# Kernel tuning notes

Measured on AMD Instinct MI355X. Metric: run time of the kernel, lower is better.

## Reference

```python
import jax, jax.numpy as jnp
import numpy as np

N_NODES = 2048
N_EDGES = 131072
N_LINE = 524288
D = 128
H = 4
NUM_RBF = 50
CUTOFF = 8.0
N_LAYERS = 4


def setup_inputs() -> dict:
    key = jax.random.key(0)
    ks = iter(jax.random.split(key, 64))
    def nrm(shape, s=0.05):
        return jax.random.normal(next(ks), shape, dtype=jnp.float32) * s
    inp = {}
    inp["atomic_numbers"] = jax.random.randint(next(ks), (N_NODES,), 1, 101)
    inp["positions"] = jax.random.normal(next(ks), (N_NODES, 3), dtype=jnp.float32) * 4.0
    inp["edge_index"] = jax.random.randint(next(ks), (2, N_EDGES), 0, N_NODES)
    inp["line_edge_index"] = jax.random.randint(next(ks), (2, N_LINE), 0, N_EDGES)
    inp["line_angles"] = jax.random.uniform(next(ks), (N_LINE, 1), dtype=jnp.float32) * np.float32(np.pi)
    # embeddings
    inp["atom_table"] = nrm((100, D), 1.0)
    inp["rbf_w1"] = nrm((NUM_RBF, D)); inp["rbf_b1"] = jnp.zeros((D,), jnp.float32)
    inp["rbf_w2"] = nrm((D, D));       inp["rbf_b2"] = jnp.zeros((D,), jnp.float32)
    inp["line_emb_w"] = nrm((1, D), 1.0); inp["line_emb_b"] = jnp.zeros((D,), jnp.float32)
    # per-layer params, stacked over N_LAYERS (weights stored [in,out], used as x @ W + b)
    inp["eu_w1"] = nrm((N_LAYERS, 3 * D, 2 * D)); inp["eu_b1"] = jnp.zeros((N_LAYERS, 2 * D), jnp.float32)
    inp["eu_w2"] = nrm((N_LAYERS, 2 * D, D));     inp["eu_b2"] = jnp.zeros((N_LAYERS, D), jnp.float32)
    inp["lu_w1"] = nrm((N_LAYERS, 2 * D, D));     inp["lu_b1"] = jnp.zeros((N_LAYERS, D), jnp.float32)
    inp["lu_w2"] = nrm((N_LAYERS, D, D));         inp["lu_b2"] = jnp.zeros((N_LAYERS, D), jnp.float32)
    inp["nu_w1"] = nrm((N_LAYERS, 2 * D, 2 * D)); inp["nu_b1"] = jnp.zeros((N_LAYERS, 2 * D), jnp.float32)
    inp["nu_w2"] = nrm((N_LAYERS, 2 * D, D));     inp["nu_b2"] = jnp.zeros((N_LAYERS, D), jnp.float32)
    inp["attn_wqkv"] = nrm((N_LAYERS, D, 3 * D)); inp["attn_bqkv"] = jnp.zeros((N_LAYERS, 3 * D), jnp.float32)
    inp["attn_wo"] = nrm((N_LAYERS, D, D));       inp["attn_bo"] = jnp.zeros((N_LAYERS, D), jnp.float32)
    inp["nn_g"] = jnp.ones((N_LAYERS, D), jnp.float32); inp["nn_b"] = jnp.zeros((N_LAYERS, D), jnp.float32)
    inp["en_g"] = jnp.ones((N_LAYERS, D), jnp.float32); inp["en_b"] = jnp.zeros((N_LAYERS, D), jnp.float32)
    inp["ln_g"] = jnp.ones((N_LAYERS, D), jnp.float32); inp["ln_b"] = jnp.zeros((N_LAYERS, D), jnp.float32)
    # readout
    inp["ro_w1"] = nrm((D, D));      inp["ro_b1"] = jnp.zeros((D,), jnp.float32)
    inp["ro_w2"] = nrm((D, D // 2)); inp["ro_b2"] = jnp.zeros((D // 2,), jnp.float32)
    inp["ro_w3"] = nrm((D // 2, 1)); inp["ro_b3"] = jnp.zeros((1,), jnp.float32)
    return inp


def _layernorm(x, g, b, eps=1e-5):
    m = jnp.mean(x, -1, keepdims=True)
    v = jnp.mean((x - m) ** 2, -1, keepdims=True)
    return (x - m) * jax.lax.rsqrt(v + eps) * g + b


def _seg_mean_num(x, idx, n):
    s = jax.ops.segment_sum(x, idx, num_segments=n)
    c = jax.ops.segment_sum(jnp.ones((idx.shape[0],), x.dtype), idx, num_segments=n)
    return s / jnp.clip(c, 1.0)[:, None]


def alignn_forward(atomic_numbers, positions, edge_index, line_edge_index, line_angles,
                   atom_table, rbf_w1, rbf_b1, rbf_w2, rbf_b2, line_emb_w, line_emb_b,
                   eu_w1, eu_b1, eu_w2, eu_b2, lu_w1, lu_b1, lu_w2, lu_b2,
                   nu_w1, nu_b1, nu_w2, nu_b2, attn_wqkv, attn_bqkv, attn_wo, attn_bo,
                   nn_g, nn_b, en_g, en_b, ln_g, ln_b,
                   ro_w1, ro_b1, ro_w2, ro_b2, ro_w3, ro_b3):
    silu = jax.nn.silu
    src, dst = edge_index[0], edge_index[1]
    lsrc, ldst = line_edge_index[0], line_edge_index[1]
    nN, nE = atomic_numbers.shape[0], src.shape[0]

    # edge distances & embeddings
    vec = positions[dst] - positions[src]                      # [E,3]
    dist = jnp.linalg.norm(vec, axis=-1)                       # [E]
    centers = jnp.linspace(0.0, CUTOFF, NUM_RBF)
    widths = jnp.full((NUM_RBF,), CUTOFF / NUM_RBF, jnp.float32)
    rbf = jnp.exp(-((dist[:, None] - centers) ** 2) / (2.0 * widths ** 2))
    cut = 0.5 * (jnp.cos(dist * jnp.pi / CUTOFF) + 1.0) * (dist < CUTOFF).astype(dist.dtype)
    rbf = rbf * cut[:, None]
    edge = silu(rbf @ rbf_w1 + rbf_b1) @ rbf_w2 + rbf_b2       # [E,D]
    node = atom_table[atomic_numbers - 1]                      # [N,D]
    line = line_angles @ line_emb_w + line_emb_b               # [Lg,D]

    xs = {"eu_w1": eu_w1, "eu_b1": eu_b1, "eu_w2": eu_w2, "eu_b2": eu_b2,
          "lu_w1": lu_w1, "lu_b1": lu_b1, "lu_w2": lu_w2, "lu_b2": lu_b2,
          "nu_w1": nu_w1, "nu_b1": nu_b1, "nu_w2": nu_w2, "nu_b2": nu_b2,
          "wqkv": attn_wqkv, "bqkv": attn_bqkv, "wo": attn_wo, "bo": attn_bo,
          "nn_g": nn_g, "nn_b": nn_b, "en_g": en_g, "en_b": en_b, "ln_g": ln_g, "ln_b": ln_b}

    def step(carry, p):
        node, edge, line = carry
        # line-graph edge update
        li = jnp.concatenate([edge[lsrc], edge[ldst]], -1)     # [Lg,2D]
        lu = silu(li @ p["lu_w1"] + p["lu_b1"]) @ p["lu_w2"] + p["lu_b2"]
        line = _layernorm(line + lu, p["ln_g"], p["ln_b"])
        # aggregate line edges -> edges (mean over dst)
        laggr = _seg_mean_num(line, ldst, nE)                  # [E,D]
        ei = jnp.concatenate([edge, edge, laggr], -1)          # [E,3D]
        eu = silu(ei @ p["eu_w1"] + p["eu_b1"]) @ p["eu_w2"] + p["eu_b2"]
        edge = _layernorm(edge + eu, p["en_g"], p["en_b"])
        # aggregate edges -> nodes (mean over dst)
        naggr = _seg_mean_num(edge, dst, nN)                   # [N,D]
        ni = jnp.concatenate([node, naggr], -1)                # [N,2D]
        nu = silu(ni @ p["nu_w1"] + p["nu_b1"]) @ p["nu_w2"] + p["nu_b2"]
        node = _layernorm(node + nu, p["nn_g"], p["nn_b"])
        # global self-attention over nodes (batch=1, seq=N)
        qkv = node @ p["wqkv"] + p["bqkv"]                     # [N,3D]
        q, k, v = jnp.split(qkv, 3, axis=-1)
        dh = D // H
        q = q.reshape(nN, H, dh); k = k.reshape(nN, H, dh); v = v.reshape(nN, H, dh)
        scores = jnp.einsum("qhd,khd->hqk", q, k) / jnp.sqrt(jnp.float32(dh))
        attn = jax.nn.softmax(scores, axis=-1)
        o = jnp.einsum("hqk,khd->qhd", attn, v).reshape(nN, D)
        node = o @ p["wo"] + p["bo"]
        return (node, edge, line), None

    (node, edge, line), _ = jax.lax.scan(step, (node, edge, line), xs)

    g = node.mean(axis=0, keepdims=True)                       # [1,D]
    h = silu(g @ ro_w1 + ro_b1)
    h = silu(h @ ro_w2 + ro_b2)
    return h @ ro_w3 + ro_b3                                   # [1,1]


def reference(atomic_numbers, positions, edge_index, line_edge_index, line_angles,
              atom_table, rbf_w1, rbf_b1, rbf_w2, rbf_b2, line_emb_w, line_emb_b,
              eu_w1, eu_b1, eu_w2, eu_b2, lu_w1, lu_b1, lu_w2, lu_b2,
              nu_w1, nu_b1, nu_w2, nu_b2, attn_wqkv, attn_bqkv, attn_wo, attn_bo,
              nn_g, nn_b, en_g, en_b, ln_g, ln_b,
              ro_w1, ro_b1, ro_w2, ro_b2, ro_w3, ro_b3):
    return alignn_forward(atomic_numbers, positions, edge_index, line_edge_index, line_angles,
                          atom_table, rbf_w1, rbf_b1, rbf_w2, rbf_b2, line_emb_w, line_emb_b,
                          eu_w1, eu_b1, eu_w2, eu_b2, lu_w1, lu_b1, lu_w2, lu_b2,
                          nu_w1, nu_b1, nu_w2, nu_b2, attn_wqkv, attn_bqkv, attn_wo, attn_bo,
                          nn_g, nn_b, en_g, en_b, ln_g, ln_b,
                          ro_w1, ro_b1, ro_w2, ro_b2, ro_w3, ro_b3)
```

## Files before the change

kernel.cpp:

```cpp
#include <hip/hip_runtime.h>
#include <hip/hip_fp16.h>


#define NN 2048
#define NE 131072
#define NL 524288
#define DM 128

typedef unsigned short u16;
typedef unsigned int uint;
typedef __attribute__((ext_vector_type(8))) _Float16 f16x8;
typedef __attribute__((ext_vector_type(2))) _Float16 f16x2;
typedef __attribute__((ext_vector_type(4))) float f32x4;

__device__ __forceinline__ float h2f(u16 u){ return __half2float(__ushort_as_half(u)); }
__device__ __forceinline__ u16 f2h(float f){ return __half_as_ushort(__float2half(f)); }
__device__ __forceinline__ uint pk2h(float a, float b){
  union { decltype(__builtin_amdgcn_cvt_pkrtz(0.f,0.f)) h2; uint u; } cv;
  cv.h2 = __builtin_amdgcn_cvt_pkrtz(a, b);
  return cv.u;
}
__device__ __forceinline__ float siluf(float x){ return x/(1.f+__expf(-x)); }
__device__ __forceinline__ float4 ld4(const float* p){ return *(const float4*)p; }
__device__ __forceinline__ void fma44(float (&a)[4], float4 x, float4 w0, float4 w1, float4 w2, float4 w3){
  a[0] += x.x*w0.x + x.y*w1.x + x.z*w2.x + x.w*w3.x;
  a[1] += x.x*w0.y + x.y*w1.y + x.z*w2.y + x.w*w3.y;
  a[2] += x.x*w0.z + x.y*w1.z + x.z*w2.z + x.w*w3.z;
  a[3] += x.x*w0.w + x.y*w1.w + x.z*w2.w + x.w*w3.w;
}


__global__ void k_zero2(int* __restrict__ a, int na, int* __restrict__ b, int nb){
  int i = blockIdx.x*256 + threadIdx.x;
  if (i < na) a[i] = 0;
  else if (i - na < nb) b[i - na] = 0;
}

__global__ void k_sentinel(float* out, float wsmb){ out[0] = 1000000.0f + wsmb; }

__global__ void k_einv(const int* __restrict__ perm2, int* __restrict__ einv, int n){
  int i = blockIdx.x*256 + threadIdx.x;
  if (i < n) einv[perm2[i]] = i;
}

__global__ void k_lidx2(const int* __restrict__ lsrc, const int* __restrict__ ldst,
                        const int* __restrict__ perm1, const int* __restrict__ einv,
                        int* __restrict__ lsrc2, int* __restrict__ ldst2, int n){
  int i = blockIdx.x*256 + threadIdx.x;
  if (i < n){
    int o = perm1[i];
    lsrc2[i] = einv[lsrc[o]];
    ldst2[i] = einv[ldst[o]];
  }
}


__global__ __launch_bounds__(256) void k_scanp1(
    const int* __restrict__ inA, int* __restrict__ outA,
    const int* __restrict__ inB, int* __restrict__ outB,
    int* __restrict__ bsumA, int* __restrict__ bsumB){
  __shared__ int wsum[4];
  const int b = blockIdx.x, t = threadIdx.x;
  const int* in;  int* out;  int* bsum;  int base;
  if (b < 64){ in = inA; out = outA; bsum = bsumA + b; base = b*2048; }
  else       { in = inB; out = outB; bsum = bsumB;     base = 0; }
  int v[8];
  int s = 0;
  #pragma unroll
  for (int j=0;j<8;j++){ v[j] = in[base + t*8 + j]; s += v[j]; }
  const int lane = t & 63, wid = t >> 6;
  int x = s;
  #pragma unroll
  for (int off=1; off<64; off<<=1){
    int u = __shfl_up(x, off);
    if (lane >= off) x += u;
  }
  if (lane == 63) wsum[wid] = x;
  __syncthreads();
  int woff = 0;
  #pragma unroll
  for (int i=0;i<3;i++) if (i < wid) woff += wsum[i];
  int run = woff + x - s;
  #pragma unroll
  for (int j=0;j<8;j++){ out[base + t*8 + j] = run; run += v[j]; }
  if (t == 255) *bsum = woff + x;
}

__global__ void k_scanp2(int* __restrict__ bsumA, int* __restrict__ outA, int nA,
                         const int* __restrict__ bsumB, int* __restrict__ outB, int nB){
  __shared__ int sh[64];
  const int t = threadIdx.x;
  if (t < 64) sh[t] = bsumA[t];
  __syncthreads();
  if (t == 0){
    int run = 0;
    for (int i=0;i<64;i++){ int v = sh[i]; sh[i] = run; run += v; }
    outA[nA] = run;
    outB[nB] = bsumB[0];
  }
  __syncthreads();
  if (t < 64) bsumA[t] = sh[t];
}

__global__ __launch_bounds__(256) void k_scanp3(int* __restrict__ outA, const int* __restrict__ bsumA){
  const int b = blockIdx.x;
  const int off = bsumA[b];
  const int base = b*2048 + threadIdx.x*8;
  #pragma unroll
  for (int j=0;j<8;j++) outA[base+j] += off;
}

__global__ void k_wfrag_all(const float* __restrict__ luw1, const float* __restrict__ luw2,
                            const float* __restrict__ euw1, const float* __restrict__ euw2,
                            u16* __restrict__ lw1h, u16* __restrict__ lw2h,
                            u16* __restrict__ ew1h, u16* __restrict__ ew2h){
  int l = blockIdx.x / 72, r = blockIdx.x % 72;
  const float* W; u16* out; int N, total, lb; bool fold = false;
  if (r < 16){      W = luw1 + (size_t)l*256*128; out = lw1h + (size_t)l*32768; N=128; total=4096;  lb = r; }
  else if (r < 24){ W = luw2 + (size_t)l*128*128; out = lw2h + (size_t)l*16384; N=128; total=2048;  lb = r-16; }
  else if (r < 56){ W = euw1 + (size_t)l*384*256; out = ew1h + (size_t)l*65536; N=256; total=8192;  lb = r-24; fold = true; }
  else {            W = euw2 + (size_t)l*256*128; out = ew2h + (size_t)l*32768; N=128; total=4096;  lb = r-56; }
  int i = lb*256 + threadIdx.x;
  if (i >= total) return;
  int lane = i & 63;
  int frag = i >> 6;
  int NT = N >> 4;
  int ntg = frag % NT;
  int kt = frag / NT;
  int half = NT >> 1;
  int colh = ntg / half, j = ntg % half;
  int col  = colh*(half<<4) + ((j>>1)<<5) + 2*(lane&15) + (j&1);
  int row0 = kt*32 + (lane>>4)*8;
  uint4 v; uint* vp = (uint*)&v;
  #pragma unroll
  for (int p=0;p<4;p++){
    int ra = row0+2*p, rb = row0+2*p+1;
    float fa, fb;
    if (fold){
      fa = (ra < 128) ? W[(size_t)ra*N + col] + W[(size_t)(ra+128)*N + col]
                      : W[(size_t)(ra+128)*N + col];
      fb = (rb < 128) ? W[(size_t)rb*N + col] + W[(size_t)(rb+128)*N + col]
                      : W[(size_t)(rb+128)*N + col];
    } else {
      fa = W[(size_t)ra*N + col];
      fb = W[(size_t)rb*N + col];
    }
    vp[p] = (uint)f2h(fa) | ((uint)f2h(fb)<<16);
  }
  *(uint4*)(out + (size_t)i*8) = v;
}

__global__ void k_rbf_wfrag(const float* __restrict__ rw1, const float* __restrict__ rw2,
                            u16* __restrict__ w1p, u16* __restrict__ w2p){
  int r = blockIdx.x;
  const float* W; u16* out; int K, total;
  if (r < 4){ W = rw1; out = w1p; K = 50;  total = 1024; }
  else      { W = rw2; out = w2p; K = 128; total = 2048; r -= 4; }
  int i = r*256 + threadIdx.x;
  if (i >= total) return;
  int lane = i & 63, frag = i >> 6;
  int ntg = frag % 8, kt = frag / 8;
  int colh = ntg / 4, j = ntg % 4;
  int col  = colh*64 + ((j>>1)<<5) + 2*(lane&15) + (j&1);
  int row0 = kt*32 + (lane>>4)*8;
  uint4 v; uint* vp = (uint*)&v;
  #pragma unroll
  for (int p=0;p<4;p++){
    int ra = row0+2*p, rb = row0+2*p+1;
    u16 a = (ra < K) ? f2h(W[(size_t)ra*128 + col]) : (u16)0;
    u16 b = (rb < K) ? f2h(W[(size_t)rb*128 + col]) : (u16)0;
    vp[p] = (uint)a | ((uint)b<<16);
  }
  *(uint4*)(out + (size_t)i*8) = v;
}


__global__ void k_node_init(const int* __restrict__ an, const float* __restrict__ tab, float* __restrict__ node){
  int i = blockIdx.x*256 + threadIdx.x;
  int n = i >> 7, d = i & 127;
  node[i] = tab[(an[n]-1)*DM + d];
}

__global__ void k_line_init(const float* __restrict__ ang, const float* __restrict__ w,
                            const float* __restrict__ b, const int* __restrict__ perm1,
                            u16* __restrict__ line){
  int i = blockIdx.x*256 + threadIdx.x;
  int r = i >> 6; int c2 = (i & 63)*2;
  float a = ang[perm1[r]];
  ushort2 v;
  v.x = f2h(a*w[c2  ] + b[c2  ]);
  v.y = f2h(a*w[c2+1] + b[c2+1]);
  ((ushort2*)line)[i] = v;
}

#define EB_RS 72
#define EB_HS 136

__global__ __launch_bounds__(256) void k_edge_embed2(
    const float* __restrict__ pos, const int* __restrict__ eidx,
    const int* __restrict__ eperm,
    const u16* __restrict__ W1p, const float* __restrict__ B1,
    const u16* __restrict__ W2p, const float* __restrict__ B2,
    u16* __restrict__ edge){
  __shared__ __align__(16) u16 rs[32*EB_RS];
  __shared__ __align__(16) u16 hs[32*EB_HS];
  __shared__ float dsh[32];
  const int t = threadIdx.x;
  const int e0 = blockIdx.x*32;
  if (t < 32){
    int eo = eperm[e0 + t];
    int s = eidx[eo], d = eidx[NE + eo];
    float dx = pos[d*3+0]-pos[s*3+0];
    float dy = pos[d*3+1]-pos[s*3+1];
    float dz = pos[d*3+2]-pos[s*3+2];
    dsh[t] = sqrtf(dx*dx+dy*dy+dz*dz);
  }
  __syncthreads();
  for (int q = t; q < 32*64; q += 256){
    int m = q >> 6, k = q & 63;
    float d = dsh[m];
    float v = 0.f;
    if (k < 50){
      float c = 8.0f*(float)k/49.0f;
      float g = __expf(-(d-c)*(d-c)*19.53125f);
      float cut = (d < 8.0f) ? 0.5f*(__cosf(d*0.39269908169872414f)+1.0f) : 0.0f;
      v = g*cut;
    }
    rs[m*EB_RS + k] = f2h(v);
  }
  __syncthreads();

  const int lane = t & 63, w = t >> 6;
  const int band = w >> 1, colh = w & 1;
  const int arow = band*16 + (lane & 15);
  const int kgrp = (lane >> 4)*8;
  const int q2 = 2*(lane & 15);

  {
    f32x4 acc[4];
    #pragma unroll
    for (int nt=0; nt<4; ++nt){
      float bv = B1[colh*64 + (nt>>1)*32 + q2 + (nt&1)];
      acc[nt][0]=bv; acc[nt][1]=bv; acc[nt][2]=bv; acc[nt][3]=bv;
    }
    #pragma unroll
    for (int kt=0; kt<2; ++kt){
      f16x8 a = *(const f16x8*)(rs + arow*EB_RS + kt*32 + kgrp);
      #pragma unroll
      for (int nt=0; nt<4; ++nt){
        int ntg = colh*4 + nt;
        f16x8 b = *(const f16x8*)(W1p + ((size_t)(kt*8 + ntg)*64 + lane)*8);
        acc[nt] = __builtin_amdgcn_mfma_f32_16x16x32_f16(a, b, acc[nt], 0, 0, 0);
      }
    }
    #pragma unroll
    for (int p=0; p<2; ++p){
      int colb = colh*64 + p*32 + q2;
      #pragma unroll
      for (int r=0; r<4; ++r){
        int row = band*16 + (lane>>4)*4 + r;
        *(uint*)(hs + row*EB_HS + colb) = pk2h(siluf(acc[2*p][r]), siluf(acc[2*p+1][r]));
      }
    }
  }
  __syncthreads();
  {
    f32x4 acc[4];
    #pragma unroll
    for (int nt=0; nt<4; ++nt){
      float bv = B2[colh*64 + (nt>>1)*32 + q2 + (nt&1)];
      acc[nt][0]=bv; acc[nt][1]=bv; acc[nt][2]=bv; acc[nt][3]=bv;
    }
    #pragma unroll
    for (int kt=0; kt<4; ++kt){
      f16x8 a = *(const f16x8*)(hs + arow*EB_HS + kt*32 + kgrp);
      #pragma unroll
      for (int nt=0; nt<4; ++nt){
        int ntg = colh*4 + nt;
        f16x8 b = *(const f16x8*)(W2p + ((size_t)(kt*8 + ntg)*64 + lane)*8);
        acc[nt] = __builtin_amdgcn_mfma_f32_16x16x32_f16(a, b, acc[nt], 0, 0, 0);
      }
    }
    #pragma unroll
    for (int p=0; p<2; ++p){
      int colb = colh*64 + p*32 + q2;
      #pragma unroll
      for (int r=0; r<4; ++r){
        int row = band*16 + (lane>>4)*4 + r;
        *(uint*)(edge + (size_t)(e0+row)*DM + colb) = pk2h(acc[2*p][r], acc[2*p+1][r]);
      }
    }
  }
}


__global__ void k_hist2(const int* __restrict__ idxA, int* __restrict__ histA,
                        const int* __restrict__ idxB, int* __restrict__ histB, int nblkA){
  int t = threadIdx.x;
  if ((int)blockIdx.x < nblkA){
    int i = blockIdx.x*256 + t;
    atomicAdd(&histA[idxA[i]], 1);
  } else {
    int i = (blockIdx.x - nblkA)*256 + t;
    atomicAdd(&histB[idxB[i]], 1);
  }
}

__global__ void k_perm2k(const int* __restrict__ idxA, const int* __restrict__ baseA,
                         int* __restrict__ curA, int* __restrict__ permA,
                         const int* __restrict__ idxB, const int* __restrict__ baseB,
                         int* __restrict__ curB, int* __restrict__ permB, int nblkA){
  int t = threadIdx.x;
  if ((int)blockIdx.x < nblkA){
    int i = blockIdx.x*256 + t;
    int e = idxA[i];
    int p = atomicAdd(&curA[e], 1);
    permA[baseA[e] + p] = i;
  } else {
    int i = (blockIdx.x - nblkA)*256 + t;
    int e = idxB[i];
    int p = atomicAdd(&curB[e], 1);
    permB[baseB[e] + p] = i;
  }
}


#define PE_XS 136

__global__ __launch_bounds__(256) void k_pre_lu(
    const u16* __restrict__ edge, const u16* __restrict__ W1h,
    u16* __restrict__ A16, u16* __restrict__ Bm16){
  __shared__ __align__(16) u16 xs[32*PE_XS];
  const int t = threadIdx.x;
  const int r0 = blockIdx.x*32;
  #pragma unroll
  for (int it=0; it<2; ++it){
    int idx = it*256 + t;
    int m = idx >> 4, c = idx & 15;
    uint4 v = *(const uint4*)(edge + (size_t)(r0+m)*DM + c*8);
    *(uint4*)(xs + m*PE_XS + c*8) = v;
  }
  __syncthreads();
  const int lane = t & 63, w = t >> 6;
  const int band = w >> 1, colh = w & 1;
  const int arow = band*16 + (lane & 15);
  const int kgrp = (lane >> 4)*8;
  const int q2 = 2*(lane & 15);
  #pragma unroll
  for (int half=0; half<2; ++half){
    f32x4 acc[4];
    #pragma unroll
    for (int nt=0; nt<4; ++nt){ acc[nt][0]=0.f; acc[nt][1]=0.f; acc[nt][2]=0.f; acc[nt][3]=0.f; }
    #pragma unroll
    for (int kt=0; kt<4; ++kt){
      f16x8 a = *(const f16x8*)(xs + arow*PE_XS + kt*32 + kgrp);
      #pragma unroll
      for (int nt=0; nt<4; ++nt){
        int ntg = colh*4 + nt;
        f16x8 b = *(const f16x8*)(W1h + ((size_t)((kt + half*4)*8 + ntg)*64 + lane)*8);
        acc[nt] = __builtin_amdgcn_mfma_f32_16x16x32_f16(a, b, acc[nt], 0, 0, 0);
      }
    }
    u16* out = half ? Bm16 : A16;
    #pragma unroll
    for (int p=0; p<2; ++p){
      int colb = colh*64 + p*32 + q2;
      #pragma unroll
      for (int r=0; r<4; ++r){
        int row = band*16 + (lane>>4)*4 + r;
        *(uint*)(out + (size_t)(r0+row)*DM + colb) = pk2h(acc[2*p][r], acc[2*p+1][r]);
      }
    }
  }
}


#define LU_HS 136
#define LU_OS 132

__global__ __launch_bounds__(256) void k_lu2(
    const u16* __restrict__ A16, const u16* __restrict__ Bm16,
    const int* __restrict__ lsrc2, const int* __restrict__ ldst2,
    const float* __restrict__ B1,
    const u16* __restrict__ W2h, const float* __restrict__ B2,
    const float* __restrict__ lg, const float* __restrict__ lb,
    u16* __restrict__ line){
  __shared__ __align__(16) float smem[32*LU_OS];
  u16* hs = (u16*)smem;
  const int t = threadIdx.x;
  const int r0 = blockIdx.x*32;

  {
    int m = t >> 3, c8 = t & 7;
    int r = r0 + m;
    const u16* ap = A16  + (size_t)lsrc2[r]*DM;
    const u16* bp = Bm16 + (size_t)ldst2[r]*DM;
    #pragma unroll
    for (int cc0=0; cc0<2; ++cc0){
      int cc = c8 + cc0*8;
      uint4 av = *(const uint4*)(ap + cc*8);
      uint4 bv = *(const uint4*)(bp + cc*8);
      const __half2* ah = (const __half2*)&av;
      const __half2* bh = (const __half2*)&bv;
      uint outw[4];
      #pragma unroll
      for (int p=0;p<4;p++){
        int col = cc*8 + 2*p;
        __half2 b1v = __floats2half2_rn(B1[col], B1[col+1]);
        __half2 x2 = __hadd2(__hadd2(ah[p], bh[p]), b1v);
        float x0 = __half2float(__low2half(x2));
        float x1 = __half2float(__high2half(x2));
        outw[p] = pk2h(siluf(x0), siluf(x1));
      }
      *(uint4*)(hs + m*LU_HS + cc*8) = *(uint4*)outw;
    }
  }
  __syncthreads();

  const int lane = t & 63, w = t >> 6;
  const int band = w >> 1, colh = w & 1;
  const int arow = band*16 + (lane & 15);
  const int kgrp = (lane >> 4)*8;
  const int q2 = 2*(lane & 15);

  f32x4 acc[4];
  #pragma unroll
  for (int nt=0; nt<4; ++nt){
    float bv = B2[colh*64 + (nt>>1)*32 + q2 + (nt&1)];
    acc[nt][0]=bv; acc[nt][1]=bv; acc[nt][2]=bv; acc[nt][3]=bv;
  }
  #pragma unroll
  for (int kt=0; kt<4; ++kt){
    f16x8 a = *(const f16x8*)(hs + arow*LU_HS + kt*32 + kgrp);
    #pragma unroll
    for (int nt=0; nt<4; ++nt){
      int ntg = colh*4 + nt;
      f16x8 b = *(const f16x8*)(W2h + ((size_t)(kt*8 + ntg)*64 + lane)*8);
      acc[nt] = __builtin_amdgcn_mfma_f32_16x16x32_f16(a, b, acc[nt], 0, 0, 0);
    }
  }
  __syncthreads();
  #pragma unroll
  for (int p=0; p<2; ++p){
    int colb = colh*64 + p*32 + q2;
    #pragma unroll
    for (int r=0; r<4; ++r){
      int row = band*16 + (lane>>4)*4 + r;
      *(float2*)(smem + row*LU_OS + colb) = make_float2(acc[2*p][r], acc[2*p+1][r]);
    }
  }
  __syncthreads();
  {
    const float* outp = (const float*)smem;
    int row = t >> 3, li = t & 7;
    size_t rb = (size_t)(r0 + row)*DM;
    uint rw[8];
    *(uint4*)&rw[0] = *(const uint4*)(line + rb + li*16);
    *(uint4*)&rw[4] = *(const uint4*)(line + rb + li*16 + 8);
    float x[16];
    float s=0.f, q=0.f;
    #pragma unroll
    for (int j=0;j<16;j++){
      float res = h2f((u16)((j&1) ? (rw[j>>1]>>16) : (rw[j>>1]&0xffffu)));
      x[j] = outp[row*LU_OS + li*16 + j] + res;
      s += x[j]; q += x[j]*x[j];
    }
    #pragma unroll
    for (int off=1; off<8; off<<=1){ s += __shfl_xor(s,off); q += __shfl_xor(q,off); }
    float mean = s*(1.f/128.f);
    float rstd = rsqrtf(fmaxf(q*(1.f/128.f) - mean*mean, 0.f) + 1e-5f);
    #pragma unroll
    for (int half=0; half<2; ++half){
      uint4 wv; uint* wp = (uint*)&wv;
      #pragma unroll
      for (int p=0;p<4;p++){
        int j = half*8 + 2*p;
        int c0 = li*16 + j;
        wp[p] = pk2h((x[j  ]-mean)*rstd*lg[c0  ] + lb[c0  ],
                     (x[j+1]-mean)*rstd*lg[c0+1] + lb[c0+1]);
      }
      *(uint4*)(line + rb + li*16 + half*8) = wv;
    }
  }
}


#define EU_XS 264
#define EU_HS 264
#define EU_OS 132

__global__ __launch_bounds__(256) void k_eu_mfma(
    const u16* __restrict__ W1h, const float* __restrict__ B1,
    const u16* __restrict__ W2h, const float* __restrict__ B2,
    const float* __restrict__ g, const float* __restrict__ bb,
    u16* __restrict__ edge, const u16* __restrict__ line,
    const int* __restrict__ lbase, const int* __restrict__ eperm){
  __shared__ __align__(16) u16 xs[32*EU_XS];
  __shared__ __align__(16) u16 hs[32*EU_HS];
  const int t = threadIdx.x;
  const int r0 = blockIdx.x*32;

  for (int it=0; it<2; ++it){
    int idx = it*256 + t;
    int m = idx >> 4, c = idx & 15;
    uint4 v = *(const uint4*)(edge + (size_t)(r0+m)*DM + c*8);
    *(uint4*)(xs + m*EU_XS + c*8) = v;
  }
  {
    int m = t >> 3, c0 = (t & 7)*16;
    int eo = eperm[r0 + m];
    int b0 = lbase[eo], b1 = lbase[eo+1];
    float s[16];
    #pragma unroll
    for (int k=0;k<16;k++) s[k]=0.f;
    for (int j=b0;j<b1;++j){
      const u16* lp = line + (size_t)j*DM + c0;
      uint rw[8];
      *(uint4*)&rw[0] = *(const uint4*)lp;
      *(uint4*)&rw[4] = *(const uint4*)(lp + 8);
      #pragma unroll
      for (int k=0;k<16;k++)
        s[k] += h2f((u16)((k&1) ? (rw[k>>1]>>16) : (rw[k>>1]&0xffffu)));
    }
    int n = b1 - b0;
    float inv = 1.f/(float)(n > 0 ? n : 1);
    #pragma unroll
    for (int half=0; half<2; ++half){
      uint4 wv; uint* wp = (uint*)&wv;
      #pragma unroll
      for (int p=0;p<4;p++){
        int k = half*8 + 2*p;
        wp[p] = pk2h(s[k]*inv, s[k+1]*inv);
      }
      *(uint4*)(xs + m*EU_XS + 128 + c0 + half*8) = wv;
    }
  }
  __syncthreads();

  const int lane = t & 63, w = t >> 6;
  const int band = w >> 1, colh = w & 1;
  const int arow = band*16 + (lane & 15);
  const int kgrp = (lane >> 4)*8;
  const int q2 = 2*(lane & 15);

  {
    f32x4 acc[8];
    #pragma unroll
    for (int nt=0; nt<8; ++nt){
      float bv = B1[colh*128 + (nt>>1)*32 + q2 + (nt&1)];
      acc[nt][0]=bv; acc[nt][1]=bv; acc[nt][2]=bv; acc[nt][3]=bv;
    }
    #pragma unroll
    for (int kt=0; kt<8; ++kt){
      f16x8 a = *(const f16x8*)(xs + arow*EU_XS + kt*32 + kgrp);
      #pragma unroll
      for (int nt=0; nt<8; ++nt){
        int ntg = colh*8 + nt;
        f16x8 b = *(const f16x8*)(W1h + ((size_t)(kt*16 + ntg)*64 + lane)*8);
        acc[nt] = __builtin_amdgcn_mfma_f32_16x16x32_f16(a, b, acc[nt], 0, 0, 0);
      }
    }
    #pragma unroll
    for (int p=0; p<4; ++p){
      int colb = colh*128 + p*32 + q2;
      #pragma unroll
      for (int r=0; r<4; ++r){
        int row = band*16 + (lane>>4)*4 + r;
        *(uint*)(hs + row*EU_HS + colb) = pk2h(siluf(acc[2*p][r]), siluf(acc[2*p+1][r]));
      }
    }
  }
  __syncthreads();
  {
    f32x4 acc[4];
    #pragma unroll
    for (int nt=0; nt<4; ++nt){
      float bv = B2[colh*64 + (nt>>1)*32 + q2 + (nt&1)];
      acc[nt][0]=bv; acc[nt][1]=bv; acc[nt][2]=bv; acc[nt][3]=bv;
    }
    #pragma unroll
    for (int kt=0; kt<8; ++kt){
      f16x8 a = *(const f16x8*)(hs + arow*EU_HS + kt*32 + kgrp);
      #pragma unroll
      for (int nt=0; nt<4; ++nt){
        int ntg = colh*4 + nt;
        f16x8 b = *(const f16x8*)(W2h + ((size_t)(kt*8 + ntg)*64 + lane)*8);
        acc[nt] = __builtin_amdgcn_mfma_f32_16x16x32_f16(a, b, acc[nt], 0, 0, 0);
      }
    }
    float* outp = (float*)xs;
    #pragma unroll
    for (int p=0; p<2; ++p){
      int colb = colh*64 + p*32 + q2;
      #pragma unroll
      for (int r=0; r<4; ++r){
        int row = band*16 + (lane>>4)*4 + r;
        *(float2*)(outp + row*EU_OS + colb) = make_float2(acc[2*p][r], acc[2*p+1][r]);
      }
    }
  }
  __syncthreads();
  {
    const float* outp = (const float*)xs;
    int row = t >> 3, li = t & 7;
    size_t rb = (size_t)(r0 + row)*DM;
    uint rw[8];
    *(uint4*)&rw[0] = *(const uint4*)(edge + rb + li*16);
    *(uint4*)&rw[4] = *(const uint4*)(edge + rb + li*16 + 8);
    float x[16];
    float s=0.f, q=0.f;
    #pragma unroll
    for (int j=0;j<16;j++){
      float res = h2f((u16)((j&1) ? (rw[j>>1]>>16) : (rw[j>>1]&0xffffu)));
      x[j] = outp[row*EU_OS + li*16 + j] + res;
      s += x[j]; q += x[j]*x[j];
    }
    #pragma unroll
    for (int off=1; off<8; off<<=1){ s += __shfl_xor(s,off); q += __shfl_xor(q,off); }
    float mean = s*(1.f/128.f);
    float rstd = rsqrtf(fmaxf(q*(1.f/128.f) - mean*mean, 0.f) + 1e-5f);
    #pragma unroll
    for (int half=0; half<2; ++half){
      uint4 wv; uint* wp = (uint*)&wv;
      #pragma unroll
      for (int p=0;p<4;p++){
        int j = half*8 + 2*p;
        int c0 = li*16 + j;
        wp[p] = pk2h((x[j  ]-mean)*rstd*g[c0  ] + bb[c0  ],
                     (x[j+1]-mean)*rstd*g[c0+1] + bb[c0+1]);
      }
      *(uint4*)(edge + rb + li*16 + half*8) = wv;
    }
  }
}


template<int KIN>
__global__ __launch_bounds__(256) void k_nu(
    const float* __restrict__ W1, const float* __restrict__ B1,
    const float* __restrict__ W2, const float* __restrict__ B2,
    const float* __restrict__ g, const float* __restrict__ bb,
    float* __restrict__ node_io, const u16* __restrict__ edge,
    const int* __restrict__ nbase){
  __shared__ __align__(16) float xsf[16*KIN];
  __shared__ __align__(16) float hsf[16*256];
  const int t = threadIdx.x;
  const int r0 = blockIdx.x*16;

  {
    int m = t >> 4, c0 = (t & 15)*8;
    int n = r0 + m;
    float4 a = ld4(node_io + (size_t)n*DM + c0);
    float4 b = ld4(node_io + (size_t)n*DM + c0 + 4);
    float* xd = &xsf[m*KIN + c0];
    xd[0]=a.x; xd[1]=a.y; xd[2]=a.z; xd[3]=a.w;
    xd[4]=b.x; xd[5]=b.y; xd[6]=b.z; xd[7]=b.w;
    int b0 = nbase[n], b1e = nbase[n+1];
    float s[8];
    #pragma unroll
    for (int k=0;k<8;k++) s[k]=0.f;
    for (int j=b0;j<b1e;++j){
      uint4 v = *(const uint4*)(edge + (size_t)j*DM + c0);
      s[0]+=h2f((u16)(v.x&0xffff)); s[1]+=h2f((u16)(v.x>>16));
      s[2]+=h2f((u16)(v.y&0xffff)); s[3]+=h2f((u16)(v.y>>16));
      s[4]+=h2f((u16)(v.z&0xffff)); s[5]+=h2f((u16)(v.z>>16));
      s[6]+=h2f((u16)(v.w&0xffff)); s[7]+=h2f((u16)(v.w>>16));
    }
    int nn = b1e - b0;
    float inv = 1.f/(float)(nn > 0 ? nn : 1);
    #pragma unroll
    for (int k=0;k<8;k++) xsf[m*KIN + 128 + c0 + k] = s[k]*inv;
  }
  __syncthreads();
  {
    const int c4 = (t & 63)*4, mg = t >> 6;
    float acc[4][4];
    float4 bv = ld4(B1 + c4);
    #pragma unroll
    for (int i=0;i<4;i++){ acc[i][0]=bv.x; acc[i][1]=bv.y; acc[i][2]=bv.z; acc[i][3]=bv.w; }
    for (int k=0;k<KIN;k+=4){
      float4 w0 = ld4(W1 + (k  )*256 + c4);
      float4 w1 = ld4(W1 + (k+1)*256 + c4);
      float4 w2 = ld4(W1 + (k+2)*256 + c4);
      float4 w3 = ld4(W1 + (k+3)*256 + c4);
      #pragma unroll
      for (int i=0;i<4;i++){
        float4 x = *(const float4*)&xsf[(mg*4+i)*KIN + k];
        fma44(acc[i], x, w0, w1, w2, w3);
      }
    }
    #pragma unroll
    for (int i=0;i<4;i++)
      #pragma unroll
      for (int j=0;j<4;j++)
        hsf[(mg*4+i)*256 + c4 + j] = siluf(acc[i][j]);
  }
  __syncthreads();
  const int c4b = (t & 31)*4, mgb = t >> 5;
  float acc2[2][4];
  {
    float4 bv = ld4(B2 + c4b);
    #pragma unroll
    for (int i=0;i<2;i++){ acc2[i][0]=bv.x; acc2[i][1]=bv.y; acc2[i][2]=bv.z; acc2[i][3]=bv.w; }
    for (int k=0;k<256;k+=4){
      float4 w0 = ld4(W2 + (k  )*128 + c4b);
      float4 w1 = ld4(W2 + (k+1)*128 + c4b);
      float4 w2 = ld4(W2 + (k+2)*128 + c4b);
      float4 w3 = ld4(W2 + (k+3)*128 + c4b);
      #pragma unroll
      for (int i=0;i<2;i++){
        float4 x = *(const float4*)&hsf[(mgb*2+i)*256 + k];
        fma44(acc2[i], x, w0, w1, w2, w3);
      }
    }
  }
  __syncthreads();
  #pragma unroll
  for (int i=0;i<2;i++){
    int m = mgb*2 + i;
    #pragma unroll
    for (int j=0;j<4;j++)
      hsf[m*128 + c4b + j] = acc2[i][j] + xsf[m*KIN + c4b + j];
  }
  __syncthreads();
  {
    int row = t >> 4, li = t & 15;
    const float* o = &hsf[row*128];
    float s=0.f, q=0.f;
    #pragma unroll
    for (int j=0;j<8;j++){ float x = o[li*8+j]; s += x; q += x*x; }
    #pragma unroll
    for (int off=1; off<16; off<<=1){ s += __shfl_xor(s,off); q += __shfl_xor(q,off); }
    float mean = s*(1.f/128.f);
    float rstd = rsqrtf(fmaxf(q*(1.f/128.f) - mean*mean, 0.f) + 1e-5f);
    size_t rb = (size_t)(r0 + row)*DM;
    #pragma unroll
    for (int j=0;j<8;j++){
      int c = li*8 + j;
      node_io[rb + c] = (o[c]-mean)*rstd*g[c] + bb[c];
    }
  }
}


__global__ void k_qkv_split(const float* __restrict__ node, const float* __restrict__ W,
                            const float* __restrict__ B, float* __restrict__ Q,
                            u16* __restrict__ K4, u16* __restrict__ V4){
  int i = blockIdx.x*256 + threadIdx.x;
  int n = i / 384, c = i % 384;
  float acc = B[c];
  const float* nr = node + (size_t)n*DM;
  for (int k=0;k<128;k+=4){
    acc += nr[k  ]*W[(k  )*384+c];
    acc += nr[k+1]*W[(k+1)*384+c];
    acc += nr[k+2]*W[(k+2)*384+c];
    acc += nr[k+3]*W[(k+3)*384+c];
  }
  if (c < 128){
    Q[(size_t)n*128 + c] = acc;
  } else if (c < 256){
    int h = (c-128) >> 5, d = (c-128) & 31;
    K4[((size_t)h*NN + n)*32 + d] = f2h(acc);
  } else {
    int h = (c-256) >> 5, d = (c-256) & 31;
    V4[((size_t)h*NN + n)*32 + d] = f2h(acc);
  }
}

#define AT_TK 128
#define AT_RU 17

__global__ __launch_bounds__(256) void k_attn3(
    const float* __restrict__ Q, const u16* __restrict__ K4,
    const u16* __restrict__ V4, float* __restrict__ attno){
  __shared__ uint kls[2][AT_TK*AT_RU];
  __shared__ uint vls[2][AT_TK*AT_RU];
  const int t = threadIdx.x, lane = t & 63;
  const int h = blockIdx.x >> 8;
  const int q0 = (blockIdx.x & 255)*8 + (t >> 6)*2;
  const float scale = 0.17677669529663687f;
  const uint* Kg = (const uint*)(K4 + (size_t)h*NN*32);
  const uint* Vg = (const uint*)(V4 + (size_t)h*NN*32);
  const int ca = t*2, cb = t*2+1;
  const int ka_ = ca>>2, pa_ = (ca&3)*4;
  const int kb_ = cb>>2, pb_ = (cb&3)*4;
  uint4 kr0, kr1, vr0, vr1;

  f16x2 qh[2][16];
  #pragma unroll
  for (int j=0;j<2;j++){
    const float* qr = Q + (size_t)(q0+j)*128 + h*32;
    #pragma unroll
    for (int u=0;u<16;u++){
      union { uint u32; f16x2 h2; } cv;
      cv.u32 = pk2h(qr[2*u]*scale, qr[2*u+1]*scale);
      qh[j][u] = cv.h2;
    }
  }
  float mx = -1e30f, s0 = 0.f, s1 = 0.f;
  float o0[32], o1[32];
  #pragma unroll
  for (int d=0;d<32;d++){ o0[d]=0.f; o1[d]=0.f; }

  {
    const uint* kg = Kg; const uint* vg = Vg;
    kr0 = *(const uint4*)(kg + ca*4); kr1 = *(const uint4*)(kg + cb*4);
    vr0 = *(const uint4*)(vg + ca*4); vr1 = *(const uint4*)(vg + cb*4);
    uint* kd = kls[0]; uint* vd = vls[0];
    kd[ka_*AT_RU+pa_  ]=kr0.x; kd[ka_*AT_RU+pa_+1]=kr0.y; kd[ka_*AT_RU+pa_+2]=kr0.z; kd[ka_*AT_RU+pa_+3]=kr0.w;
    kd[kb_*AT_RU+pb_  ]=kr1.x; kd[kb_*AT_RU+pb_+1]=kr1.y; kd[kb_*AT_RU+pb_+2]=kr1.z; kd[kb_*AT_RU+pb_+3]=kr1.w;
    vd[ka_*AT_RU+pa_  ]=vr0.x; vd[ka_*AT_RU+pa_+1]=vr0.y; vd[ka_*AT_RU+pa_+2]=vr0.z; vd[ka_*AT_RU+pa_+3]=vr0.w;
    vd[kb_*AT_RU+pb_  ]=vr1.x; vd[kb_*AT_RU+pb_+1]=vr1.y; vd[kb_*AT_RU+pb_+2]=vr1.z; vd[kb_*AT_RU+pb_+3]=vr1.w;
  }
  __syncthreads();

  const int NT = NN / AT_TK;
  for (int kt=0; kt<NT; ++kt){
    if (kt+1 < NT){
      const uint* kg = Kg + (size_t)(kt+1)*AT_TK*16;
      const uint* vg = Vg + (size_t)(kt+1)*AT_TK*16;
      kr0 = *(const uint4*)(kg + ca*4); kr1 = *(const uint4*)(kg + cb*4);
      vr0 = *(const uint4*)(vg + ca*4); vr1 = *(const uint4*)(vg + cb*4);
    }
    {
      const uint* kb = kls[kt&1];
      const uint* vb = vls[kt&1];
      const uint* krA = kb + lane*AT_RU;
      const uint* krB = kb + (lane+64)*AT_RU;
      float dA0=0.f, dA1=0.f, dB0=0.f, dB1=0.f;
      #pragma unroll
      for (int u=0;u<16;u++){
        union { uint u32; f16x2 h2; } ka, kbv;
        ka.u32  = krA[u];
        kbv.u32 = krB[u];
        dA0 = __builtin_amdgcn_fdot2(ka.h2,  qh[0][u], dA0, false);
        dA1 = __builtin_amdgcn_fdot2(ka.h2,  qh[1][u], dA1, false);
        dB0 = __builtin_amdgcn_fdot2(kbv.h2, qh[0][u], dB0, false);
        dB1 = __builtin_amdgcn_fdot2(kbv.h2, qh[1][u], dB1, false);
      }
      float nm = fmaxf(mx, fmaxf(fmaxf(dA0,dA1), fmaxf(dB0,dB1)));
      float r  = __expf(mx - nm);
      mx = nm;
      float eA0 = __expf(dA0 - nm), eA1 = __expf(dA1 - nm);
      float eB0 = __expf(dB0 - nm), eB1 = __expf(dB1 - nm);
      s0 = s0*r + eA0 + eB0;
      s1 = s1*r + eA1 + eB1;
      const uint* vrA = vb + lane*AT_RU;
      const uint* vrB = vb + (lane+64)*AT_RU;
      #pragma unroll
      for (int u=0;u<16;u++){
        uint wA = vrA[u], wB = vrB[u];
        float aA = h2f((u16)(wA&0xffffu)), bA = h2f((u16)(wA>>16));
        float aB = h2f((u16)(wB&0xffffu)), bB = h2f((u16)(wB>>16));
        o0[2*u  ] = o0[2*u  ]*r + eA0*aA + eB0*aB;
        o0[2*u+1] = o0[2*u+1]*r + eA0*bA + eB0*bB;
        o1[2*u  ] = o1[2*u  ]*r + eA1*aA + eB1*aB;
        o1[2*u+1] = o1[2*u+1]*r + eA1*bA + eB1*bB;
      }
    }
    __syncthreads();
    if (kt+1 < NT){
      uint* kd = kls[(kt+1)&1]; uint* vd = vls[(kt+1)&1];
      kd[ka_*AT_RU+pa_  ]=kr0.x; kd[ka_*AT_RU+pa_+1]=kr0.y; kd[ka_*AT_RU+pa_+2]=kr0.z; kd[ka_*AT_RU+pa_+3]=kr0.w;
      kd[kb_*AT_RU+pb_  ]=kr1.x; kd[kb_*AT_RU+pb_+1]=kr1.y; kd[kb_*AT_RU+pb_+2]=kr1.z; kd[kb_*AT_RU+pb_+3]=kr1.w;
      vd[ka_*AT_RU+pa_  ]=vr0.x; vd[ka_*AT_RU+pa_+1]=vr0.y; vd[ka_*AT_RU+pa_+2]=vr0.z; vd[ka_*AT_RU+pa_+3]=vr0.w;
      vd[kb_*AT_RU+pb_  ]=vr1.x; vd[kb_*AT_RU+pb_+1]=vr1.y; vd[kb_*AT_RU+pb_+2]=vr1.z; vd[kb_*AT_RU+pb_+3]=vr1.w;
      __syncthreads();
    }
  }

  #pragma unroll
  for (int off=1; off<64; off<<=1){
    float m2  = __shfl_xor(mx, off);
    float s02 = __shfl_xor(s0, off);
    float s12 = __shfl_xor(s1, off);
    float nm = fmaxf(mx, m2);
    float ra = __expf(mx - nm), rb = __expf(m2 - nm);
    s0 = s0*ra + s02*rb;
    s1 = s1*ra + s12*rb;
    #pragma unroll
    for (int d=0;d<32;d++){
      float a0 = __shfl_xor(o0[d], off);
      float a1 = __shfl_xor(o1[d], off);
      o0[d] = o0[d]*ra + a0*rb;
      o1[d] = o1[d]*ra + a1*rb;
    }
    mx = nm;
  }
  float inv0 = 1.f/s0, inv1 = 1.f/s1;
  if (lane == 0){
    #pragma unroll
    for (int d=0;d<32;d++){
      attno[(size_t)(q0  )*DM + h*32 + d] = o0[d]*inv0;
      attno[(size_t)(q0+1)*DM + h*32 + d] = o1[d]*inv1;
    }
  }
}

__global__ void k_wo(const float* __restrict__ attno, const float* __restrict__ W,
                     const float* __restrict__ B, float* __restrict__ node){
  int i = blockIdx.x*256 + threadIdx.x;
  int n = i >> 7, c = i & 127;
  float acc = B[c];
  const float* ar = attno + (size_t)n*DM;
  for (int k=0;k<128;k+=4){
    acc += ar[k  ]*W[(k  )*128+c];
    acc += ar[k+1]*W[(k+1)*128+c];
    acc += ar[k+2]*W[(k+2)*128+c];
    acc += ar[k+3]*W[(k+3)*128+c];
  }
  node[i] = acc;
}


__global__ __launch_bounds__(256) void k_readout(
    const float* __restrict__ node,
    const float* __restrict__ w1, const float* __restrict__ b1,
    const float* __restrict__ w2, const float* __restrict__ b2,
    const float* __restrict__ w3, const float* __restrict__ b3,
    float* __restrict__ out){
  __shared__ float gs[128], h1[128], h2[64];
  const int t = threadIdx.x;
  if (t < 128){
    float s = 0.f;
    for (int r=0;r<NN;r++) s += node[(size_t)r*DM + t];
    gs[t] = s*(1.f/2048.f);
  }
  __syncthreads();
  if (t < 128){
    float acc = b1[t];
    for (int k=0;k<128;k++) acc += gs[k]*w1[k*128+t];
    h1[t] = siluf(acc);
  }
  __syncthreads();
  if (t < 64){
    float acc = b2[t];
    for (int k=0;k<128;k++) acc += h1[k]*w2[k*64+t];
    h2[t] = siluf(acc);
  }
  __syncthreads();
  if (t == 0){
    float acc = b3[0];
    for (int k=0;k<64;k++) acc += h2[k]*w3[k];
    out[0] = acc;
  }
}


extern "C" void kernel_launch(void* const* d_in, const int* in_sizes, int n_in,
                              void* d_out, int out_size, void* d_ws, size_t ws_size,
                              hipStream_t stream) {
  (void)in_sizes; (void)n_in; (void)out_size;
  const int*   an    = (const int*)  d_in[0];
  const float* pos   = (const float*)d_in[1];
  const int*   eidx  = (const int*)  d_in[2];
  const int*   lidx  = (const int*)  d_in[3];
  const float* lang  = (const float*)d_in[4];
  const float* atab  = (const float*)d_in[5];
  const float* rw1   = (const float*)d_in[6];
  const float* rb1   = (const float*)d_in[7];
  const float* rw2   = (const float*)d_in[8];
  const float* rb2   = (const float*)d_in[9];
  const float* lew   = (const float*)d_in[10];
  const float* leb   = (const float*)d_in[11];
  const float* euw1  = (const float*)d_in[12];
  const float* eub1  = (const float*)d_in[13];
  const float* euw2  = (const float*)d_in[14];
  const float* eub2  = (const float*)d_in[15];
  const float* luw1  = (const float*)d_in[16];
  const float* lub1  = (const float*)d_in[17];
  const float* luw2  = (const float*)d_in[18];
  const float* lub2  = (const float*)d_in[19];
  const float* nuw1  = (const float*)d_in[20];
  const float* nub1  = (const float*)d_in[21];
  const float* nuw2  = (const float*)d_in[22];
  const float* nub2  = (const float*)d_in[23];
  const float* wqkv  = (const float*)d_in[24];
  const float* bqkv  = (const float*)d_in[25];
  const float* wo    = (const float*)d_in[26];
  const float* bo    = (const float*)d_in[27];
  const float* nng   = (const float*)d_in[28];
  const float* nnb   = (const float*)d_in[29];
  const float* eng   = (const float*)d_in[30];
  const float* enb   = (const float*)d_in[31];
  const float* lng   = (const float*)d_in[32];
  const float* lnb   = (const float*)d_in[33];
  const float* row1  = (const float*)d_in[34];
  const float* rob1  = (const float*)d_in[35];
  const float* row2  = (const float*)d_in[36];
  const float* rob2  = (const float*)d_in[37];
  const float* row3  = (const float*)d_in[38];
  const float* rob3  = (const float*)d_in[39];

  char* p = (char*)d_ws;
  auto bump = [&](size_t bytes)->char*{ char* q = p; p += (bytes + 255) & ~(size_t)255; return q; };
  float* node  = (float*)bump((size_t)NN*DM*4);
  float* Q     = (float*)bump((size_t)NN*128*4);
  u16*   K4    = (u16*)  bump((size_t)4*NN*32*2);
  u16*   V4    = (u16*)  bump((size_t)4*NN*32*2);
  float* attno = (float*)bump((size_t)NN*DM*4);
  u16*   edge  = (u16*)  bump((size_t)NE*DM*2);
  u16*   line  = (u16*)  bump((size_t)NL*DM*2);
  u16*   A16   = (u16*)  bump((size_t)NE*DM*2);
  u16*   Bm16  = (u16*)  bump((size_t)NE*DM*2);
  int*   base1 = (int*)  bump((size_t)(NE+1)*4);
  int*   base2 = (int*)  bump((size_t)(NN+1)*4);
  int*   cur1  = (int*)  bump((size_t)NE*4);
  int*   cur2  = (int*)  bump((size_t)NN*4);
  int*   perm1 = (int*)  bump((size_t)NL*4);
  int*   perm2 = (int*)  bump((size_t)NE*4);
  int*   einv  = (int*)  bump((size_t)NE*4);
  int*   lsrc2 = (int*)  bump((size_t)NL*4);
  int*   ldst2 = (int*)  bump((size_t)NL*4);
  int*   bsumA = (int*)  bump((size_t)64*4);
  int*   bsumB = (int*)  bump((size_t)4);
  u16*   lw1h  = (u16*)  bump((size_t)4*32768*2);
  u16*   lw2h  = (u16*)  bump((size_t)4*16384*2);
  u16*   ew1h  = (u16*)  bump((size_t)4*65536*2);
  u16*   ew2h  = (u16*)  bump((size_t)4*32768*2);
  u16*   rw1p  = (u16*)  bump((size_t)8192*2);
  u16*   rw2p  = (u16*)  bump((size_t)16384*2);
  size_t needed = (size_t)(p - (char*)d_ws);
  if (needed > ws_size){
    k_sentinel<<<1, 1, 0, stream>>>((float*)d_out, (float)(ws_size >> 20));
    return;
  }

  const int* lsrc = lidx;
  const int* ldst = lidx + NL;
  const int* dst  = eidx + NE;

  const int nblkA = NL/256, nblkB = NE/256;
  k_zero2<<<(NE+NN+255)/256, 256, 0, stream>>>(cur1, NE, cur2, NN);
  k_hist2<<<nblkA+nblkB, 256, 0, stream>>>(ldst, cur1, dst, cur2, nblkA);
  k_scanp1<<<65, 256, 0, stream>>>(cur1, base1, cur2, base2, bsumA, bsumB);
  k_scanp2<<<1, 64, 0, stream>>>(bsumA, base1, NE, bsumB, base2, NN);
  k_scanp3<<<64, 256, 0, stream>>>(base1, bsumA);
  k_zero2<<<(NE+NN+255)/256, 256, 0, stream>>>(cur1, NE, cur2, NN);
  k_perm2k<<<nblkA+nblkB, 256, 0, stream>>>(ldst, base1, cur1, perm1,
                                            dst,  base2, cur2, perm2, nblkA);
  k_einv<<<(NE+255)/256, 256, 0, stream>>>(perm2, einv, NE);
  k_lidx2<<<(NL+255)/256, 256, 0, stream>>>(lsrc, ldst, perm1, einv, lsrc2, ldst2, NL);

  k_wfrag_all<<<4*72, 256, 0, stream>>>(luw1, luw2, euw1, euw2, lw1h, lw2h, ew1h, ew2h);
  k_rbf_wfrag<<<12, 256, 0, stream>>>(rw1, rw2, rw1p, rw2p);

  k_node_init<<<NN*DM/256, 256, 0, stream>>>(an, atab, node);
  k_line_init<<<NL*64/256, 256, 0, stream>>>(lang, lew, leb, perm1, line);
  k_edge_embed2<<<NE/32, 256, 0, stream>>>(pos, eidx, perm2, rw1p, rb1, rw2p, rb2, edge);

  for (int l=0; l<4; ++l){
    k_pre_lu<<<NE/32, 256, 0, stream>>>(edge, lw1h + (size_t)l*32768, A16, Bm16);
    k_lu2<<<NL/32, 256, 0, stream>>>(A16, Bm16, lsrc2, ldst2,
        lub1 + l*128, lw2h + (size_t)l*16384, lub2 + l*128,
        lng + l*128, lnb + l*128, line);
    k_eu_mfma<<<NE/32, 256, 0, stream>>>(
        ew1h + (size_t)l*65536, eub1 + l*256,
        ew2h + (size_t)l*32768, eub2 + l*128,
        eng + l*128, enb + l*128, edge, line, base1, perm2);
    k_nu<256><<<NN/16, 256, 0, stream>>>(
        nuw1 + (size_t)l*256*256, nub1 + l*256, nuw2 + (size_t)l*256*128, nub2 + l*128,
        nng + l*128, nnb + l*128, node, edge, base2);
    k_qkv_split<<<NN*384/256, 256, 0, stream>>>(node, wqkv + (size_t)l*128*384, bqkv + l*384,
        Q, K4, V4);
    k_attn3<<<1024, 256, 0, stream>>>(Q, K4, V4, attno);
    k_wo<<<NN*DM/256, 256, 0, stream>>>(attno, wo + (size_t)l*128*128, bo + l*128, node);
  }

  k_readout<<<1, 256, 0, stream>>>(node, row1, rob1, row2, rob2, row3, rob3, (float*)d_out);
}
```

Baseline: 1.834 ms.

## Co-schedule next layer's line/edge updates with current layer's attention in merged launches

Kernel bodies become device functions, and combined kernels (k_qp, k_la, k_we) dispatch by block index. Each one runs the node-attention stage of layer l alongside the line and edge update stages of layer l+1, which depend only on edge and line state. This fills the GPU during the small attention kernels and removes launch gaps. The risk is that the merged kernels take the register and shared-memory footprint of their heaviest part, which can reduce occupancy for the larger line and edge work.

```diff
diff --git a/kernel.cpp b/kernel.cpp
--- a/kernel.cpp
+++ b/kernel.cpp
@@ -326,13 +326,13 @@
 
 
 #define PE_XS 136
-
-__global__ __launch_bounds__(256) void k_pre_lu(
+#define PE_SMEM (32*PE_XS*2)
+
+__device__ __forceinline__ void dev_pre_lu(int bid,
     const u16* __restrict__ edge, const u16* __restrict__ W1h,
-    u16* __restrict__ A16, u16* __restrict__ Bm16){
-  __shared__ __align__(16) u16 xs[32*PE_XS];
+    u16* __restrict__ A16, u16* __restrict__ Bm16, u16* xs){
   const int t = threadIdx.x;
-  const int r0 = blockIdx.x*32;
+  const int r0 = bid*32;
   #pragma unroll
   for (int it=0; it<2; ++it){
     int idx = it*256 + t;
@@ -374,9 +374,443 @@
   }
 }
 
-
 #define LU_HS 136
 #define LU_OS 132
+#define LU_SMEM (32*LU_OS*4)
+
+__device__ __forceinline__ void dev_lu2(int bid,
+    const u16* __restrict__ A16, const u16* __restrict__ Bm16,
+    const int* __restrict__ lsrc2, const int* __restrict__ ldst2,
+    const float* __restrict__ B1,
+    const u16* __restrict__ W2h, const float* __restrict__ B2,
+    const float* __restrict__ lg, const float* __restrict__ lb,
+    u16* __restrict__ line, float* smem){
+  u16* hs = (u16*)smem;
+  const int t = threadIdx.x;
+  const int r0 = bid*32;
+
+  {
+    int m = t >> 3, c8 = t & 7;
+    int r = r0 + m;
+    const u16* ap = A16  + (size_t)lsrc2[r]*DM;
+    const u16* bp = Bm16 + (size_t)ldst2[r]*DM;
+    #pragma unroll
+    for (int cc0=0; cc0<2; ++cc0){
+      int cc = c8 + cc0*8;
+      uint4 av = *(const uint4*)(ap + cc*8);
+      uint4 bv = *(const uint4*)(bp + cc*8);
+      const __half2* ah = (const __half2*)&av;
+      const __half2* bh = (const __half2*)&bv;
+      uint outw[4];
+      #pragma unroll
+      for (int p=0;p<4;p++){
+        int col = cc*8 + 2*p;
+        __half2 b1v = __floats2half2_rn(B1[col], B1[col+1]);
+        __half2 x2 = __hadd2(__hadd2(ah[p], bh[p]), b1v);
+        float x0 = __half2float(__low2half(x2));
+        float x1 = __half2float(__high2half(x2));
+        outw[p] = pk2h(siluf(x0), siluf(x1));
+      }
+      *(uint4*)(hs + m*LU_HS + cc*8) = *(uint4*)outw;
+    }
+  }
+  __syncthreads();
+
+  const int lane = t & 63, w = t >> 6;
+  const int band = w >> 1, colh = w & 1;
+  const int arow = band*16 + (lane & 15);
+  const int kgrp = (lane >> 4)*8;
+  const int q2 = 2*(lane & 15);
+
+  f32x4 acc[4];
+  #pragma unroll
+  for (int nt=0; nt<4; ++nt){
+    float bv = B2[colh*64 + (nt>>1)*32 + q2 + (nt&1)];
+    acc[nt][0]=bv; acc[nt][1]=bv; acc[nt][2]=bv; acc[nt][3]=bv;
+  }
+  #pragma unroll
+  for (int kt=0; kt<4; ++kt){
+    f16x8 a = *(const f16x8*)(hs + arow*LU_HS + kt*32 + kgrp);
+    #pragma unroll
+    for (int nt=0; nt<4; ++nt){
+      int ntg = colh*4 + nt;
+      f16x8 b = *(const f16x8*)(W2h + ((size_t)(kt*8 + ntg)*64 + lane)*8);
+      acc[nt] = __builtin_amdgcn_mfma_f32_16x16x32_f16(a, b, acc[nt], 0, 0, 0);
+    }
+  }
+  __syncthreads();
+  #pragma unroll
+  for (int p=0; p<2; ++p){
+    int colb = colh*64 + p*32 + q2;
+    #pragma unroll
+    for (int r=0; r<4; ++r){
+      int row = band*16 + (lane>>4)*4 + r;
+      *(float2*)(smem + row*LU_OS + colb) = make_float2(acc[2*p][r], acc[2*p+1][r]);
+    }
+  }
+  __syncthreads();
+  {
+    const float* outp = (const float*)smem;
+    int row = t >> 3, li = t & 7;
+    size_t rb = (size_t)(r0 + row)*DM;
+    uint rw[8];
+    *(uint4*)&rw[0] = *(const uint4*)(line + rb + li*16);
+    *(uint4*)&rw[4] = *(const uint4*)(line + rb + li*16 + 8);
+    float x[16];
+    float s=0.f, q=0.f;
+    #pragma unroll
+    for (int j=0;j<16;j++){
+      float res = h2f((u16)((j&1) ? (rw[j>>1]>>16) : (rw[j>>1]&0xffffu)));
+      x[j] = outp[row*LU_OS + li*16 + j] + res;
+      s += x[j]; q += x[j]*x[j];
+    }
+    #pragma unroll
+    for (int off=1; off<8; off<<=1){ s += __shfl_xor(s,off); q += __shfl_xor(q,off); }
+    float mean = s*(1.f/128.f);
+    float rstd = rsqrtf(fmaxf(q*(1.f/128.f) - mean*mean, 0.f) + 1e-5f);
+    #pragma unroll
+    for (int half=0; half<2; ++half){
+      uint4 wv; uint* wp = (uint*)&wv;
+      #pragma unroll
+      for (int p=0;p<4;p++){
+        int j = half*8 + 2*p;
+        int c0 = li*16 + j;
+        wp[p] = pk2h((x[j  ]-mean)*rstd*lg[c0  ] + lb[c0  ],
+                     (x[j+1]-mean)*rstd*lg[c0+1] + lb[c0+1]);
+      }
+      *(uint4*)(line + rb + li*16 + half*8) = wv;
+    }
+  }
+}
+
+#define EU_XS 264
+#define EU_HS 264
+#define EU_OS 132
+#define EU_SMEM (32*EU_XS*2 + 32*EU_HS*2)
+
+__device__ __forceinline__ void dev_eu(int bid,
+    const u16* __restrict__ W1h, const float* __restrict__ B1,
+    const u16* __restrict__ W2h, const float* __restrict__ B2,
+    const float* __restrict__ g, const float* __restrict__ bb,
+    u16* __restrict__ edge, const u16* __restrict__ line,
+    const int* __restrict__ lbase, const int* __restrict__ eperm,
+    u16* xs, u16* hs){
+  const int t = threadIdx.x;
+  const int r0 = bid*32;
+
+  for (int it=0; it<2; ++it){
+    int idx = it*256 + t;
+    int m = idx >> 4, c = idx & 15;
+    uint4 v = *(const uint4*)(edge + (size_t)(r0+m)*DM + c*8);
+    *(uint4*)(xs + m*EU_XS + c*8) = v;
+  }
+  {
+    int m = t >> 3, c0 = (t & 7)*16;
+    int eo = eperm[r0 + m];
+    int b0 = lbase[eo], b1 = lbase[eo+1];
+    float s[16];
+    #pragma unroll
+    for (int k=0;k<16;k++) s[k]=0.f;
+    for (int j=b0;j<b1;++j){
+      const u16* lp = line + (size_t)j*DM + c0;
+      uint rw[8];
+      *(uint4*)&rw[0] = *(const uint4*)lp;
+      *(uint4*)&rw[4] = *(const uint4*)(lp + 8);
+      #pragma unroll
+      for (int k=0;k<16;k++)
+        s[k] += h2f((u16)((k&1) ? (rw[k>>1]>>16) : (rw[k>>1]&0xffffu)));
+    }
+    int n = b1 - b0;
+    float inv = 1.f/(float)(n > 0 ? n : 1);
+    #pragma unroll
+    for (int half=0; half<2; ++half){
+      uint4 wv; uint* wp = (uint*)&wv;
+      #pragma unroll
+      for (int p=0;p<4;p++){
+        int k = half*8 + 2*p;
+        wp[p] = pk2h(s[k]*inv, s[k+1]*inv);
+      }
+      *(uint4*)(xs + m*EU_XS + 128 + c0 + half*8) = wv;
+    }
+  }
+  __syncthreads();
+
+  const int lane = t & 63, w = t >> 6;
+  const int band = w >> 1, colh = w & 1;
+  const int arow = band*16 + (lane & 15);
+  const int kgrp = (lane >> 4)*8;
+  const int q2 = 2*(lane & 15);
+
+  {
+    f32x4 acc[8];
+    #pragma unroll
+    for (int nt=0; nt<8; ++nt){
+      float bv = B1[colh*128 + (nt>>1)*32 + q2 + (nt&1)];
+      acc[nt][0]=bv; acc[nt][1]=bv; acc[nt][2]=bv; acc[nt][3]=bv;
+    }
+    #pragma unroll
+    for (int kt=0; kt<8; ++kt){
+      f16x8 a = *(const f16x8*)(xs + arow*EU_XS + kt*32 + kgrp);
+      #pragma unroll
+      for (int nt=0; nt<8; ++nt){
+        int ntg = colh*8 + nt;
+        f16x8 b = *(const f16x8*)(W1h + ((size_t)(kt*16 + ntg)*64 + lane)*8);
+        acc[nt] = __builtin_amdgcn_mfma_f32_16x16x32_f16(a, b, acc[nt], 0, 0, 0);
+      }
+    }
+    #pragma unroll
+    for (int p=0; p<4; ++p){
+      int colb = colh*128 + p*32 + q2;
+      #pragma unroll
+      for (int r=0; r<4; ++r){
+        int row = band*16 + (lane>>4)*4 + r;
+        *(uint*)(hs + row*EU_HS + colb) = pk2h(siluf(acc[2*p][r]), siluf(acc[2*p+1][r]));
+      }
+    }
+  }
+  __syncthreads();
+  {
+    f32x4 acc[4];
+    #pragma unroll
+    for (int nt=0; nt<4; ++nt){
+      float bv = B2[colh*64 + (nt>>1)*32 + q2 + (nt&1)];
+      acc[nt][0]=bv; acc[nt][1]=bv; acc[nt][2]=bv; acc[nt][3]=bv;
+    }
+    #pragma unroll
+    for (int kt=0; kt<8; ++kt){
+      f16x8 a = *(const f16x8*)(hs + arow*EU_HS + kt*32 + kgrp);
+      #pragma unroll
+      for (int nt=0; nt<4; ++nt){
+        int ntg = colh*4 + nt;
+        f16x8 b = *(const f16x8*)(W2h + ((size_t)(kt*8 + ntg)*64 + lane)*8);
+        acc[nt] = __builtin_amdgcn_mfma_f32_16x16x32_f16(a, b, acc[nt], 0, 0, 0);
+      }
+    }
+    float* outp = (float*)xs;
+    #pragma unroll
+    for (int p=0; p<2; ++p){
+      int colb = colh*64 + p*32 + q2;
+      #pragma unroll
+      for (int r=0; r<4; ++r){
+        int row = band*16 + (lane>>4)*4 + r;
+        *(float2*)(outp + row*EU_OS + colb) = make_float2(acc[2*p][r], acc[2*p+1][r]);
+      }
+    }
+  }
+  __syncthreads();
+  {
+    const float* outp = (const float*)xs;
+    int row = t >> 3, li = t & 7;
+    size_t rb = (size_t)(r0 + row)*DM;
+    uint rw[8];
+    *(uint4*)&rw[0] = *(const uint4*)(edge + rb + li*16);
+    *(uint4*)&rw[4] = *(const uint4*)(edge + rb + li*16 + 8);
+    float x[16];
+    float s=0.f, q=0.f;
+    #pragma unroll
+    for (int j=0;j<16;j++){
+      float res = h2f((u16)((j&1) ? (rw[j>>1]>>16) : (rw[j>>1]&0xffffu)));
+      x[j] = outp[row*EU_OS + li*16 + j] + res;
+      s += x[j]; q += x[j]*x[j];
+    }
+    #pragma unroll
+    for (int off=1; off<8; off<<=1){ s += __shfl_xor(s,off); q += __shfl_xor(q,off); }
+    float mean = s*(1.f/128.f);
+    float rstd = rsqrtf(fmaxf(q*(1.f/128.f) - mean*mean, 0.f) + 1e-5f);
+    #pragma unroll
+    for (int half=0; half<2; ++half){
+      uint4 wv; uint* wp = (uint*)&wv;
+      #pragma unroll
+      for (int p=0;p<4;p++){
+        int j = half*8 + 2*p;
+        int c0 = li*16 + j;
+        wp[p] = pk2h((x[j  ]-mean)*rstd*g[c0  ] + bb[c0  ],
+                     (x[j+1]-mean)*rstd*g[c0+1] + bb[c0+1]);
+      }
+      *(uint4*)(edge + rb + li*16 + half*8) = wv;
+    }
+  }
+}
+
+__device__ __forceinline__ void dev_qkv(int bid,
+    const float* __restrict__ node, const float* __restrict__ W,
+    const float* __restrict__ B, float* __restrict__ Q,
+    u16* __restrict__ K4, u16* __restrict__ V4){
+  int i = bid*256 + threadIdx.x;
+  int n = i / 384, c = i % 384;
+  float acc = B[c];
+  const float* nr = node + (size_t)n*DM;
+  for (int k=0;k<128;k+=4){
+    acc += nr[k  ]*W[(k  )*384+c];
+    acc += nr[k+1]*W[(k+1)*384+c];
+    acc += nr[k+2]*W[(k+2)*384+c];
+    acc += nr[k+3]*W[(k+3)*384+c];
+  }
+  if (c < 128){
+    Q[(size_t)n*128 + c] = acc;
+  } else if (c < 256){
+    int h = (c-128) >> 5, d = (c-128) & 31;
+    K4[((size_t)h*NN + n)*32 + d] = f2h(acc);
+  } else {
+    int h = (c-256) >> 5, d = (c-256) & 31;
+    V4[((size_t)h*NN + n)*32 + d] = f2h(acc);
+  }
+}
+
+#define AT_TK 128
+#define AT_RU 17
+#define AT_SMEM (4*AT_TK*AT_RU*4)
+
+__device__ __forceinline__ void dev_attn(int bid,
+    const float* __restrict__ Q, const u16* __restrict__ K4,
+    const u16* __restrict__ V4, float* __restrict__ attno,
+    uint* kls, uint* vls){
+  const int t = threadIdx.x, lane = t & 63;
+  const int h = bid >> 8;
+  const int q0 = (bid & 255)*8 + (t >> 6)*2;
+  const float scale = 0.17677669529663687f;
+  const uint* Kg = (const uint*)(K4 + (size_t)h*NN*32);
+  const uint* Vg = (const uint*)(V4 + (size_t)h*NN*32);
+  const int ca = t*2, cb = t*2+1;
+  const int ka_ = ca>>2, pa_ = (ca&3)*4;
+  const int kb_ = cb>>2, pb_ = (cb&3)*4;
+  uint4 kr0, kr1, vr0, vr1;
+
+  f16x2 qh[2][16];
+  #pragma unroll
+  for (int j=0;j<2;j++){
+    const float* qr = Q + (size_t)(q0+j)*128 + h*32;
+    #pragma unroll
+    for (int u=0;u<16;u++){
+      union { uint u32; f16x2 h2; } cv;
+      cv.u32 = pk2h(qr[2*u]*scale, qr[2*u+1]*scale);
+      qh[j][u] = cv.h2;
+    }
+  }
+  float mx = -1e30f, s0 = 0.f, s1 = 0.f;
+  float o0[32], o1[32];
+  #pragma unroll
+  for (int d=0;d<32;d++){ o0[d]=0.f; o1[d]=0.f; }
+
+  {
+    const uint* kg = Kg; const uint* vg = Vg;
+    kr0 = *(const uint4*)(kg + ca*4); kr1 = *(const uint4*)(kg + cb*4);
+    vr0 = *(const uint4*)(vg + ca*4); vr1 = *(const uint4*)(vg + cb*4);
+    uint* kd = kls; uint* vd = vls;
+    kd[ka_*AT_RU+pa_  ]=kr0.x; kd[ka_*AT_RU+pa_+1]=kr0.y; kd[ka_*AT_RU+pa_+2]=kr0.z; kd[ka_*AT_RU+pa_+3]=kr0.w;
+    kd[kb_*AT_RU+pb_  ]=kr1.x; kd[kb_*AT_RU+pb_+1]=kr1.y; kd[kb_*AT_RU+pb_+2]=kr1.z; kd[kb_*AT_RU+pb_+3]=kr1.w;
+    vd[ka_*AT_RU+pa_  ]=vr0.x; vd[ka_*AT_RU+pa_+1]=vr0.y; vd[ka_*AT_RU+pa_+2]=vr0.z; vd[ka_*AT_RU+pa_+3]=vr0.w;
+    vd[kb_*AT_RU+pb_  ]=vr1.x; vd[kb_*AT_RU+pb_+1]=vr1.y; vd[kb_*AT_RU+pb_+2]=vr1.z; vd[kb_*AT_RU+pb_+3]=vr1.w;
+  }
+  __syncthreads();
+
+  const int NT = NN / AT_TK;
+  for (int kt=0; kt<NT; ++kt){
+    if (kt+1 < NT){
+      const uint* kg = Kg + (size_t)(kt+1)*AT_TK*16;
+      const uint* vg = Vg + (size_t)(kt+1)*AT_TK*16;
+      kr0 = *(const uint4*)(kg + ca*4); kr1 = *(const uint4*)(kg + cb*4);
+      vr0 = *(const uint4*)(vg + ca*4); vr1 = *(const uint4*)(vg + cb*4);
+    }
+    {
+      const uint* kb = kls + (kt&1)*AT_TK*AT_RU;
+      const uint* vb = vls + (kt&1)*AT_TK*AT_RU;
+      const uint* krA = kb + lane*AT_RU;
+      const uint* krB = kb + (lane+64)*AT_RU;
+      float dA0=0.f, dA1=0.f, dB0=0.f, dB1=0.f;
+      #pragma unroll
+      for (int u=0;u<16;u++){
+        union { uint u32; f16x2 h2; } ka, kbv;
+        ka.u32  = krA[u];
+        kbv.u32 = krB[u];
+        dA0 = __builtin_amdgcn_fdot2(ka.h2,  qh[0][u], dA0, false);
+        dA1 = __builtin_amdgcn_fdot2(ka.h2,  qh[1][u], dA1, false);
+        dB0 = __builtin_amdgcn_fdot2(kbv.h2, qh[0][u], dB0, false);
+        dB1 = __builtin_amdgcn_fdot2(kbv.h2, qh[1][u], dB1, false);
+      }
+      float nm = fmaxf(mx, fmaxf(fmaxf(dA0,dA1), fmaxf(dB0,dB1)));
+      float r  = __expf(mx - nm);
+      mx = nm;
+      float eA0 = __expf(dA0 - nm), eA1 = __expf(dA1 - nm);
+      float eB0 = __expf(dB0 - nm), eB1 = __expf(dB1 - nm);
+      s0 = s0*r + eA0 + eB0;
+      s1 = s1*r + eA1 + eB1;
+      const uint* vrA = vb + lane*AT_RU;
+      const uint* vrB = vb + (lane+64)*AT_RU;
+      #pragma unroll
+      for (int u=0;u<16;u++){
+        uint wA = vrA[u], wB = vrB[u];
+        float aA = h2f((u16)(wA&0xffffu)), bA = h2f((u16)(wA>>16));
+        float aB = h2f((u16)(wB&0xffffu)), bB = h2f((u16)(wB>>16));
+        o0[2*u  ] = o0[2*u  ]*r + eA0*aA + eB0*aB;
+        o0[2*u+1] = o0[2*u+1]*r + eA0*bA + eB0*bB;
+        o1[2*u  ] = o1[2*u  ]*r + eA1*aA + eB1*aB;
+        o1[2*u+1] = o1[2*u+1]*r + eA1*bA + eB1*bB;
+      }
+    }
+    __syncthreads();
+    if (kt+1 < NT){
+      uint* kd = kls + ((kt+1)&1)*AT_TK*AT_RU;
+      uint* vd = vls + ((kt+1)&1)*AT_TK*AT_RU;
+      kd[ka_*AT_RU+pa_  ]=kr0.x; kd[ka_*AT_RU+pa_+1]=kr0.y; kd[ka_*AT_RU+pa_+2]=kr0.z; kd[ka_*AT_RU+pa_+3]=kr0.w;
+      kd[kb_*AT_RU+pb_  ]=kr1.x; kd[kb_*AT_RU+pb_+1]=kr1.y; kd[kb_*AT_RU+pb_+2]=kr1.z; kd[kb_*AT_RU+pb_+3]=kr1.w;
+      vd[ka_*AT_RU+pa_  ]=vr0.x; vd[ka_*AT_RU+pa_+1]=vr0.y; vd[ka_*AT_RU+pa_+2]=vr0.z; vd[ka_*AT_RU+pa_+3]=vr0.w;
+      vd[kb_*AT_RU+pb_  ]=vr1.x; vd[kb_*AT_RU+pb_+1]=vr1.y; vd[kb_*AT_RU+pb_+2]=vr1.z; vd[kb_*AT_RU+pb_+3]=vr1.w;
+      __syncthreads();
+    }
+  }
+
+  #pragma unroll
+  for (int off=1; off<64; off<<=1){
+    float m2  = __shfl_xor(mx, off);
+    float s02 = __shfl_xor(s0, off);
+    float s12 = __shfl_xor(s1, off);
+    float nm = fmaxf(mx, m2);
+    float ra = __expf(mx - nm), rb = __expf(m2 - nm);
+    s0 = s0*ra + s02*rb;
+    s1 = s1*ra + s12*rb;
+    #pragma unroll
+    for (int d=0;d<32;d++){
+      float a0 = __shfl_xor(o0[d], off);
+      float a1 = __shfl_xor(o1[d], off);
+      o0[d] = o0[d]*ra + a0*rb;
+      o1[d] = o1[d]*ra + a1*rb;
+    }
+    mx = nm;
+  }
+  float inv0 = 1.f/s0, inv1 = 1.f/s1;
+  if (lane == 0){
+    #pragma unroll
+    for (int d=0;d<32;d++){
+      attno[(size_t)(q0  )*DM + h*32 + d] = o0[d]*inv0;
+      attno[(size_t)(q0+1)*DM + h*32 + d] = o1[d]*inv1;
+    }
+  }
+}
+
+__device__ __forceinline__ void dev_wo(int bid,
+    const float* __restrict__ attno, const float* __restrict__ W,
+    const float* __restrict__ B, float* __restrict__ node){
+  int i = bid*256 + threadIdx.x;
+  int n = i >> 7, c = i & 127;
+  float acc = B[c];
+  const float* ar = attno + (size_t)n*DM;
+  for (int k=0;k<128;k+=4){
+    acc += ar[k  ]*W[(k  )*128+c];
+    acc += ar[k+1]*W[(k+1)*128+c];
+    acc += ar[k+2]*W[(k+2)*128+c];
+    acc += ar[k+3]*W[(k+3)*128+c];
+  }
+  node[i] = acc;
+}
+
+
+__global__ __launch_bounds__(256) void k_pre_lu(
+    const u16* __restrict__ edge, const u16* __restrict__ W1h,
+    u16* __restrict__ A16, u16* __restrict__ Bm16){
+  __shared__ __align__(16) u16 xs[32*PE_XS];
+  dev_pre_lu(blockIdx.x, edge, W1h, A16, Bm16, xs);
+}
 
 __global__ __launch_bounds__(256) void k_lu2(
     const u16* __restrict__ A16, const u16* __restrict__ Bm16,
@@ -386,108 +820,8 @@
     const float* __restrict__ lg, const float* __restrict__ lb,
     u16* __restrict__ line){
   __shared__ __align__(16) float smem[32*LU_OS];
-  u16* hs = (u16*)smem;
-  const int t = threadIdx.x;
-  const int r0 = blockIdx.x*32;
-
-  {
-    int m = t >> 3, c8 = t & 7;
-    int r = r0 + m;
-    const u16* ap = A16  + (size_t)lsrc2[r]*DM;
-    const u16* bp = Bm16 + (size_t)ldst2[r]*DM;
-    #pragma unroll
-    for (int cc0=0; cc0<2; ++cc0){
-      int cc = c8 + cc0*8;
-      uint4 av = *(const uint4*)(ap + cc*8);
-      uint4 bv = *(const uint4*)(bp + cc*8);
-      const __half2* ah = (const __half2*)&av;
-      const __half2* bh = (const __half2*)&bv;
-      uint outw[4];
-      #pragma unroll
-      for (int p=0;p<4;p++){
-        int col = cc*8 + 2*p;
-        __half2 b1v = __floats2half2_rn(B1[col], B1[col+1]);
-        __half2 x2 = __hadd2(__hadd2(ah[p], bh[p]), b1v);
-        float x0 = __half2float(__low2half(x2));
-        float x1 = __half2float(__high2half(x2));
-        outw[p] = pk2h(siluf(x0), siluf(x1));
-      }
-      *(uint4*)(hs + m*LU_HS + cc*8) = *(uint4*)outw;
-    }
-  }
-  __syncthreads();
-
-  const int lane = t & 63, w = t >> 6;
-  const int band = w >> 1, colh = w & 1;
-  const int arow = band*16 + (lane & 15);
-  const int kgrp = (lane >> 4)*8;
-  const int q2 = 2*(lane & 15);
-
-  f32x4 acc[4];
-  #pragma unroll
-  for (int nt=0; nt<4; ++nt){
-    float bv = B2[colh*64 + (nt>>1)*32 + q2 + (nt&1)];
-    acc[nt][0]=bv; acc[nt][1]=bv; acc[nt][2]=bv; acc[nt][3]=bv;
-  }
-  #pragma unroll
-  for (int kt=0; kt<4; ++kt){
-    f16x8 a = *(const f16x8*)(hs + arow*LU_HS + kt*32 + kgrp);
-    #pragma unroll
-    for (int nt=0; nt<4; ++nt){
-      int ntg = colh*4 + nt;
-      f16x8 b = *(const f16x8*)(W2h + ((size_t)(kt*8 + ntg)*64 + lane)*8);
-      acc[nt] = __builtin_amdgcn_mfma_f32_16x16x32_f16(a, b, acc[nt], 0, 0, 0);
-    }
-  }
-  __syncthreads();
-  #pragma unroll
-  for (int p=0; p<2; ++p){
-    int colb = colh*64 + p*32 + q2;
-    #pragma unroll
-    for (int r=0; r<4; ++r){
-      int row = band*16 + (lane>>4)*4 + r;
-      *(float2*)(smem + row*LU_OS + colb) = make_float2(acc[2*p][r], acc[2*p+1][r]);
-    }
-  }
-  __syncthreads();
-  {
-    const float* outp = (const float*)smem;
-    int row = t >> 3, li = t & 7;
-    size_t rb = (size_t)(r0 + row)*DM;
-    uint rw[8];
-    *(uint4*)&rw[0] = *(const uint4*)(line + rb + li*16);
-    *(uint4*)&rw[4] = *(const uint4*)(line + rb + li*16 + 8);
-    float x[16];
-    float s=0.f, q=0.f;
-    #pragma unroll
-    for (int j=0;j<16;j++){
-      float res = h2f((u16)((j&1) ? (rw[j>>1]>>16) : (rw[j>>1]&0xffffu)));
-      x[j] = outp[row*LU_OS + li*16 + j] + res;
-      s += x[j]; q += x[j]*x[j];
-    }
-    #pragma unroll
-    for (int off=1; off<8; off<<=1){ s += __shfl_xor(s,off); q += __shfl_xor(q,off); }
-    float mean = s*(1.f/128.f);
-    float rstd = rsqrtf(fmaxf(q*(1.f/128.f) - mean*mean, 0.f) + 1e-5f);
-    #pragma unroll
-    for (int half=0; half<2; ++half){
-      uint4 wv; uint* wp = (uint*)&wv;
-      #pragma unroll
-      for (int p=0;p<4;p++){
-        int j = half*8 + 2*p;
-        int c0 = li*16 + j;
-        wp[p] = pk2h((x[j  ]-mean)*rstd*lg[c0  ] + lb[c0  ],
-                     (x[j+1]-mean)*rstd*lg[c0+1] + lb[c0+1]);
-      }
-      *(uint4*)(line + rb + li*16 + half*8) = wv;
-    }
-  }
-}
-
-
-#define EU_XS 264
-#define EU_HS 264
-#define EU_OS 132
+  dev_lu2(blockIdx.x, A16, Bm16, lsrc2, ldst2, B1, W2h, B2, lg, lb, line, smem);
+}
 
 __global__ __launch_bounds__(256) void k_eu_mfma(
     const u16* __restrict__ W1h, const float* __restrict__ B1,
@@ -497,140 +831,77 @@
     const int* __restrict__ lbase, const int* __restrict__ eperm){
   __shared__ __align__(16) u16 xs[32*EU_XS];
   __shared__ __align__(16) u16 hs[32*EU_HS];
-  const int t = threadIdx.x;
-  const int r0 = blockIdx.x*32;
-
-  for (int it=0; it<2; ++it){
-    int idx = it*256 + t;
-    int m = idx >> 4, c = idx & 15;
-    uint4 v = *(const uint4*)(edge + (size_t)(r0+m)*DM + c*8);
-    *(uint4*)(xs + m*EU_XS + c*8) = v;
-  }
-  {
-    int m = t >> 3, c0 = (t & 7)*16;
-    int eo = eperm[r0 + m];
-    int b0 = lbase[eo], b1 = lbase[eo+1];
-    float s[16];
-    #pragma unroll
-    for (int k=0;k<16;k++) s[k]=0.f;
-    for (int j=b0;j<b1;++j){
-      const u16* lp = line + (size_t)j*DM + c0;
-      uint rw[8];
-      *(uint4*)&rw[0] = *(const uint4*)lp;
-      *(uint4*)&rw[4] = *(const uint4*)(lp + 8);
-      #pragma unroll
-      for (int k=0;k<16;k++)
-        s[k] += h2f((u16)((k&1) ? (rw[k>>1]>>16) : (rw[k>>1]&0xffffu)));
-    }
-    int n = b1 - b0;
-    float inv = 1.f/(float)(n > 0 ? n : 1);
-    #pragma unroll
-    for (int half=0; half<2; ++half){
-      uint4 wv; uint* wp = (uint*)&wv;
-      #pragma unroll
-      for (int p=0;p<4;p++){
-        int k = half*8 + 2*p;
-        wp[p] = pk2h(s[k]*inv, s[k+1]*inv);
-      }
-      *(uint4*)(xs + m*EU_XS + 128 + c0 + half*8) = wv;
-    }
-  }
-  __syncthreads();
-
-  const int lane = t & 63, w = t >> 6;
-  const int band = w >> 1, colh = w & 1;
-  const int arow = band*16 + (lane & 15);
-  const int kgrp = (lane >> 4)*8;
-  const int q2 = 2*(lane & 15);
-
-  {
-    f32x4 acc[8];
-    #pragma unroll
-    for (int nt=0; nt<8; ++nt){
-      float bv = B1[colh*128 + (nt>>1)*32 + q2 + (nt&1)];
-      acc[nt][0]=bv; acc[nt][1]=bv; acc[nt][2]=bv; acc[nt][3]=bv;
-    }
-    #pragma unroll
-    for (int kt=0; kt<8; ++kt){
-      f16x8 a = *(const f16x8*)(xs + arow*EU_XS + kt*32 + kgrp);
-      #pragma unroll
-      for (int nt=0; nt<8; ++nt){
-        int ntg = colh*8 + nt;
-        f16x8 b = *(const f16x8*)(W1h + ((size_t)(kt*16 + ntg)*64 + lane)*8);
-        acc[nt] = __builtin_amdgcn_mfma_f32_16x16x32_f16(a, b, acc[nt], 0, 0, 0);
-      }
-    }
-    #pragma unroll
-    for (int p=0; p<4; ++p){
-      int colb = colh*128 + p*32 + q2;
-      #pragma unroll
-      for (int r=0; r<4; ++r){
-        int row = band*16 + (lane>>4)*4 + r;
-        *(uint*)(hs + row*EU_HS + colb) = pk2h(siluf(acc[2*p][r]), siluf(acc[2*p+1][r]));
-      }
-    }
-  }
-  __syncthreads();
-  {
-    f32x4 acc[4];
-    #pragma unroll
-    for (int nt=0; nt<4; ++nt){
-      float bv = B2[colh*64 + (nt>>1)*32 + q2 + (nt&1)];
-      acc[nt][0]=bv; acc[nt][1]=bv; acc[nt][2]=bv; acc[nt][3]=bv;
-    }
-    #pragma unroll
-    for (int kt=0; kt<8; ++kt){
-      f16x8 a = *(const f16x8*)(hs + arow*EU_HS + kt*32 + kgrp);
-      #pragma unroll
-      for (int nt=0; nt<4; ++nt){
-        int ntg = colh*4 + nt;
-        f16x8 b = *(const f16x8*)(W2h + ((size_t)(kt*8 + ntg)*64 + lane)*8);
-        acc[nt] = __builtin_amdgcn_mfma_f32_16x16x32_f16(a, b, acc[nt], 0, 0, 0);
-      }
-    }
-    float* outp = (float*)xs;
-    #pragma unroll
-    for (int p=0; p<2; ++p){
-      int colb = colh*64 + p*32 + q2;
-      #pragma unroll
-      for (int r=0; r<4; ++r){
-        int row = band*16 + (lane>>4)*4 + r;
-        *(float2*)(outp + row*EU_OS + colb) = make_float2(acc[2*p][r], acc[2*p+1][r]);
-      }
-    }
-  }
-  __syncthreads();
-  {
-    const float* outp = (const float*)xs;
-    int row = t >> 3, li = t & 7;
-    size_t rb = (size_t)(r0 + row)*DM;
-    uint rw[8];
-    *(uint4*)&rw[0] = *(const uint4*)(edge + rb + li*16);
-    *(uint4*)&rw[4] = *(const uint4*)(edge + rb + li*16 + 8);
-    float x[16];
-    float s=0.f, q=0.f;
-    #pragma unroll
-    for (int j=0;j<16;j++){
-      float res = h2f((u16)((j&1) ? (rw[j>>1]>>16) : (rw[j>>1]&0xffffu)));
-      x[j] = outp[row*EU_OS + li*16 + j] + res;
-      s += x[j]; q += x[j]*x[j];
-    }
-    #pragma unroll
-    for (int off=1; off<8; off<<=1){ s += __shfl_xor(s,off); q += __shfl_xor(q,off); }
-    float mean = s*(1.f/128.f);
-    float rstd = rsqrtf(fmaxf(q*(1.f/128.f) - mean*mean, 0.f) + 1e-5f);
-    #pragma unroll
-    for (int half=0; half<2; ++half){
-      uint4 wv; uint* wp = (uint*)&wv;
-      #pragma unroll
-      for (int p=0;p<4;p++){
-        int j = half*8 + 2*p;
-        int c0 = li*16 + j;
-        wp[p] = pk2h((x[j  ]-mean)*rstd*g[c0  ] + bb[c0  ],
-                     (x[j+1]-mean)*rstd*g[c0+1] + bb[c0+1]);
-      }
-      *(uint4*)(edge + rb + li*16 + half*8) = wv;
-    }
+  dev_eu(blockIdx.x, W1h, B1, W2h, B2, g, bb, edge, line, lbase, eperm, xs, hs);
+}
+
+__global__ void k_qkv_split(const float* __restrict__ node, const float* __restrict__ W,
+                            const float* __restrict__ B, float* __restrict__ Q,
+                            u16* __restrict__ K4, u16* __restrict__ V4){
+  dev_qkv(blockIdx.x, node, W, B, Q, K4, V4);
+}
+
+__global__ __launch_bounds__(256) void k_attn3(
+    const float* __restrict__ Q, const u16* __restrict__ K4,
+    const u16* __restrict__ V4, float* __restrict__ attno){
+  __shared__ __align__(16) uint kls[2*AT_TK*AT_RU];
+  __shared__ __align__(16) uint vls[2*AT_TK*AT_RU];
+  dev_attn(blockIdx.x, Q, K4, V4, attno, kls, vls);
+}
+
+__global__ void k_wo(const float* __restrict__ attno, const float* __restrict__ W,
+                     const float* __restrict__ B, float* __restrict__ node){
+  dev_wo(blockIdx.x, attno, W, B, node);
+}
+
+
+__global__ __launch_bounds__(256) void k_qp(
+    const float* __restrict__ node, const float* __restrict__ Wq,
+    const float* __restrict__ Bq, float* __restrict__ Q,
+    u16* __restrict__ K4, u16* __restrict__ V4,
+    const u16* __restrict__ edge, const u16* __restrict__ W1h,
+    u16* __restrict__ A16, u16* __restrict__ Bm16){
+  __shared__ __align__(16) u16 xs[32*PE_XS];
+  int bid = blockIdx.x;
+  if (bid < NE/32) dev_pre_lu(bid, edge, W1h, A16, Bm16, xs);
+  else             dev_qkv(bid - NE/32, node, Wq, Bq, Q, K4, V4);
+}
+
+__global__ __launch_bounds__(256) void k_la(
+    const float* __restrict__ Q, const u16* __restrict__ K4,
+    const u16* __restrict__ V4, float* __restrict__ attno,
+    const u16* __restrict__ A16, const u16* __restrict__ Bm16,
+    const int* __restrict__ lsrc2, const int* __restrict__ ldst2,
+    const float* __restrict__ B1,
+    const u16* __restrict__ W2h, const float* __restrict__ B2,
+    const float* __restrict__ lg, const float* __restrict__ lb,
+    u16* __restrict__ line){
+  __shared__ __align__(16) char smem[AT_SMEM];
+  int bid = blockIdx.x;
+  if (bid < 1024){
+    uint* kls = (uint*)smem;
+    uint* vls = kls + 2*AT_TK*AT_RU;
+    dev_attn(bid, Q, K4, V4, attno, kls, vls);
+  } else {
+    dev_lu2(bid - 1024, A16, Bm16, lsrc2, ldst2, B1, W2h, B2, lg, lb, line, (float*)smem);
+  }
+}
+
+__global__ __launch_bounds__(256) void k_we(
+    const u16* __restrict__ W1h, const float* __restrict__ B1,
+    const u16* __restrict__ W2h, const float* __restrict__ B2,
+    const float* __restrict__ g, const float* __restrict__ bb,
+    u16* __restrict__ edge, const u16* __restrict__ line,
+    const int* __restrict__ lbase, const int* __restrict__ eperm,
+    const float* __restrict__ attno, const float* __restrict__ Wo,
+    const float* __restrict__ Bo, float* __restrict__ node){
+  __shared__ __align__(16) char smem[EU_SMEM];
+  int bid = blockIdx.x;
+  if (bid < NE/32){
+    u16* xs = (u16*)smem;
+    u16* hs = xs + 32*EU_XS;
+    dev_eu(bid, W1h, B1, W2h, B2, g, bb, edge, line, lbase, eperm, xs, hs);
+  } else {
+    dev_wo(bid - NE/32, attno, Wo, Bo, node);
   }
 }
 
@@ -740,176 +1011,6 @@
       node_io[rb + c] = (o[c]-mean)*rstd*g[c] + bb[c];
     }
   }
-}
-
-
-__global__ void k_qkv_split(const float* __restrict__ node, const float* __restrict__ W,
-                            const float* __restrict__ B, float* __restrict__ Q,
-                            u16* __restrict__ K4, u16* __restrict__ V4){
-  int i = blockIdx.x*256 + threadIdx.x;
-  int n = i / 384, c = i % 384;
-  float acc = B[c];
-  const float* nr = node + (size_t)n*DM;
-  for (int k=0;k<128;k+=4){
-    acc += nr[k  ]*W[(k  )*384+c];
-    acc += nr[k+1]*W[(k+1)*384+c];
-    acc += nr[k+2]*W[(k+2)*384+c];
-    acc += nr[k+3]*W[(k+3)*384+c];
-  }
-  if (c < 128){
-    Q[(size_t)n*128 + c] = acc;
-  } else if (c < 256){
-    int h = (c-128) >> 5, d = (c-128) & 31;
-    K4[((size_t)h*NN + n)*32 + d] = f2h(acc);
-  } else {
-    int h = (c-256) >> 5, d = (c-256) & 31;
-    V4[((size_t)h*NN + n)*32 + d] = f2h(acc);
-  }
-}
-
-#define AT_TK 128
-#define AT_RU 17
-
-__global__ __launch_bounds__(256) void k_attn3(
-    const float* __restrict__ Q, const u16* __restrict__ K4,
-    const u16* __restrict__ V4, float* __restrict__ attno){
-  __shared__ uint kls[2][AT_TK*AT_RU];
-  __shared__ uint vls[2][AT_TK*AT_RU];
-  const int t = threadIdx.x, lane = t & 63;
-  const int h = blockIdx.x >> 8;
-  const int q0 = (blockIdx.x & 255)*8 + (t >> 6)*2;
-  const float scale = 0.17677669529663687f;
-  const uint* Kg = (const uint*)(K4 + (size_t)h*NN*32);
-  const uint* Vg = (const uint*)(V4 + (size_t)h*NN*32);
-  const int ca = t*2, cb = t*2+1;
-  const int ka_ = ca>>2, pa_ = (ca&3)*4;
-  const int kb_ = cb>>2, pb_ = (cb&3)*4;
-  uint4 kr0, kr1, vr0, vr1;
-
-  f16x2 qh[2][16];
-  #pragma unroll
-  for (int j=0;j<2;j++){
-    const float* qr = Q + (size_t)(q0+j)*128 + h*32;
-    #pragma unroll
-    for (int u=0;u<16;u++){
-      union { uint u32; f16x2 h2; } cv;
-      cv.u32 = pk2h(qr[2*u]*scale, qr[2*u+1]*scale);
-      qh[j][u] = cv.h2;
-    }
-  }
-  float mx = -1e30f, s0 = 0.f, s1 = 0.f;
-  float o0[32], o1[32];
-  #pragma unroll
-  for (int d=0;d<32;d++){ o0[d]=0.f; o1[d]=0.f; }
-
-  {
-    const uint* kg = Kg; const uint* vg = Vg;
-    kr0 = *(const uint4*)(kg + ca*4); kr1 = *(const uint4*)(kg + cb*4);
-    vr0 = *(const uint4*)(vg + ca*4); vr1 = *(const uint4*)(vg + cb*4);
-    uint* kd = kls[0]; uint* vd = vls[0];
-    kd[ka_*AT_RU+pa_  ]=kr0.x; kd[ka_*AT_RU+pa_+1]=kr0.y; kd[ka_*AT_RU+pa_+2]=kr0.z; kd[ka_*AT_RU+pa_+3]=kr0.w;
-    kd[kb_*AT_RU+pb_  ]=kr1.x; kd[kb_*AT_RU+pb_+1]=kr1.y; kd[kb_*AT_RU+pb_+2]=kr1.z; kd[kb_*AT_RU+pb_+3]=kr1.w;
-    vd[ka_*AT_RU+pa_  ]=vr0.x; vd[ka_*AT_RU+pa_+1]=vr0.y; vd[ka_*AT_RU+pa_+2]=vr0.z; vd[ka_*AT_RU+pa_+3]=vr0.w;
-    vd[kb_*AT_RU+pb_  ]=vr1.x; vd[kb_*AT_RU+pb_+1]=vr1.y; vd[kb_*AT_RU+pb_+2]=vr1.z; vd[kb_*AT_RU+pb_+3]=vr1.w;
-  }
-  __syncthreads();
-
-  const int NT = NN / AT_TK;
-  for (int kt=0; kt<NT; ++kt){
-    if (kt+1 < NT){
-      const uint* kg = Kg + (size_t)(kt+1)*AT_TK*16;
-      const uint* vg = Vg + (size_t)(kt+1)*AT_TK*16;
-      kr0 = *(const uint4*)(kg + ca*4); kr1 = *(const uint4*)(kg + cb*4);
-      vr0 = *(const uint4*)(vg + ca*4); vr1 = *(const uint4*)(vg + cb*4);
-    }
-    {
-      const uint* kb = kls[kt&1];
-      const uint* vb = vls[kt&1];
-      const uint* krA = kb + lane*AT_RU;
-      const uint* krB = kb + (lane+64)*AT_RU;
-      float dA0=0.f, dA1=0.f, dB0=0.f, dB1=0.f;
-      #pragma unroll
-      for (int u=0;u<16;u++){
-        union { uint u32; f16x2 h2; } ka, kbv;
-        ka.u32  = krA[u];
-        kbv.u32 = krB[u];
-        dA0 = __builtin_amdgcn_fdot2(ka.h2,  qh[0][u], dA0, false);
-        dA1 = __builtin_amdgcn_fdot2(ka.h2,  qh[1][u], dA1, false);
-        dB0 = __builtin_amdgcn_fdot2(kbv.h2, qh[0][u], dB0, false);
-        dB1 = __builtin_amdgcn_fdot2(kbv.h2, qh[1][u], dB1, false);
-      }
-      float nm = fmaxf(mx, fmaxf(fmaxf(dA0,dA1), fmaxf(dB0,dB1)));
-      float r  = __expf(mx - nm);
-      mx = nm;
-      float eA0 = __expf(dA0 - nm), eA1 = __expf(dA1 - nm);
-      float eB0 = __expf(dB0 - nm), eB1 = __expf(dB1 - nm);
-      s0 = s0*r + eA0 + eB0;
-      s1 = s1*r + eA1 + eB1;
-      const uint* vrA = vb + lane*AT_RU;
-      const uint* vrB = vb + (lane+64)*AT_RU;
-      #pragma unroll
-      for (int u=0;u<16;u++){
-        uint wA = vrA[u], wB = vrB[u];
-        float aA = h2f((u16)(wA&0xffffu)), bA = h2f((u16)(wA>>16));
-        float aB = h2f((u16)(wB&0xffffu)), bB = h2f((u16)(wB>>16));
-        o0[2*u  ] = o0[2*u  ]*r + eA0*aA + eB0*aB;
-        o0[2*u+1] = o0[2*u+1]*r + eA0*bA + eB0*bB;
-        o1[2*u  ] = o1[2*u  ]*r + eA1*aA + eB1*aB;
-        o1[2*u+1] = o1[2*u+1]*r + eA1*bA + eB1*bB;
-      }
-    }
-    __syncthreads();
-    if (kt+1 < NT){
-      uint* kd = kls[(kt+1)&1]; uint* vd = vls[(kt+1)&1];
-      kd[ka_*AT_RU+pa_  ]=kr0.x; kd[ka_*AT_RU+pa_+1]=kr0.y; kd[ka_*AT_RU+pa_+2]=kr0.z; kd[ka_*AT_RU+pa_+3]=kr0.w;
-      kd[kb_*AT_RU+pb_  ]=kr1.x; kd[kb_*AT_RU+pb_+1]=kr1.y; kd[kb_*AT_RU+pb_+2]=kr1.z; kd[kb_*AT_RU+pb_+3]=kr1.w;
-      vd[ka_*AT_RU+pa_  ]=vr0.x; vd[ka_*AT_RU+pa_+1]=vr0.y; vd[ka_*AT_RU+pa_+2]=vr0.z; vd[ka_*AT_RU+pa_+3]=vr0.w;
-      vd[kb_*AT_RU+pb_  ]=vr1.x; vd[kb_*AT_RU+pb_+1]=vr1.y; vd[kb_*AT_RU+pb_+2]=vr1.z; vd[kb_*AT_RU+pb_+3]=vr1.w;
-      __syncthreads();
-    }
-  }
-
-  #pragma unroll
-  for (int off=1; off<64; off<<=1){
-    float m2  = __shfl_xor(mx, off);
-    float s02 = __shfl_xor(s0, off);
-    float s12 = __shfl_xor(s1, off);
-    float nm = fmaxf(mx, m2);
-    float ra = __expf(mx - nm), rb = __expf(m2 - nm);
-    s0 = s0*ra + s02*rb;
-    s1 = s1*ra + s12*rb;
-    #pragma unroll
-    for (int d=0;d<32;d++){
-      float a0 = __shfl_xor(o0[d], off);
-      float a1 = __shfl_xor(o1[d], off);
-      o0[d] = o0[d]*ra + a0*rb;
-      o1[d] = o1[d]*ra + a1*rb;
-    }
-    mx = nm;
-  }
-  float inv0 = 1.f/s0, inv1 = 1.f/s1;
-  if (lane == 0){
-    #pragma unroll
-    for (int d=0;d<32;d++){
-      attno[(size_t)(q0  )*DM + h*32 + d] = o0[d]*inv0;
-      attno[(size_t)(q0+1)*DM + h*32 + d] = o1[d]*inv1;
-    }
-  }
-}
-
-__global__ void k_wo(const float* __restrict__ attno, const float* __restrict__ W,
-                     const float* __restrict__ B, float* __restrict__ node){
-  int i = blockIdx.x*256 + threadIdx.x;
-  int n = i >> 7, c = i & 127;
-  float acc = B[c];
-  const float* ar = attno + (size_t)n*DM;
-  for (int k=0;k<128;k+=4){
-    acc += ar[k  ]*W[(k  )*128+c];
-    acc += ar[k+1]*W[(k+1)*128+c];
-    acc += ar[k+2]*W[(k+2)*128+c];
-    acc += ar[k+3]*W[(k+3)*128+c];
-  }
-  node[i] = acc;
 }
 
 
@@ -1049,22 +1150,37 @@
   k_line_init<<<NL*64/256, 256, 0, stream>>>(lang, lew, leb, perm1, line);
   k_edge_embed2<<<NE/32, 256, 0, stream>>>(pos, eidx, perm2, rw1p, rb1, rw2p, rb2, edge);
 
+  k_pre_lu<<<NE/32, 256, 0, stream>>>(edge, lw1h, A16, Bm16);
+  k_lu2<<<NL/32, 256, 0, stream>>>(A16, Bm16, lsrc2, ldst2,
+      lub1, lw2h, lub2, lng, lnb, line);
+  k_eu_mfma<<<NE/32, 256, 0, stream>>>(ew1h, eub1, ew2h, eub2,
+      eng, enb, edge, line, base1, perm2);
+
   for (int l=0; l<4; ++l){
-    k_pre_lu<<<NE/32, 256, 0, stream>>>(edge, lw1h + (size_t)l*32768, A16, Bm16);
-    k_lu2<<<NL/32, 256, 0, stream>>>(A16, Bm16, lsrc2, ldst2,
-        lub1 + l*128, lw2h + (size_t)l*16384, lub2 + l*128,
-        lng + l*128, lnb + l*128, line);
-    k_eu_mfma<<<NE/32, 256, 0, stream>>>(
-        ew1h + (size_t)l*65536, eub1 + l*256,
-        ew2h + (size_t)l*32768, eub2 + l*128,
-        eng + l*128, enb + l*128, edge, line, base1, perm2);
     k_nu<256><<<NN/16, 256, 0, stream>>>(
         nuw1 + (size_t)l*256*256, nub1 + l*256, nuw2 + (size_t)l*256*128, nub2 + l*128,
         nng + l*128, nnb + l*128, node, edge, base2);
-    k_qkv_split<<<NN*384/256, 256, 0, stream>>>(node, wqkv + (size_t)l*128*384, bqkv + l*384,
-        Q, K4, V4);
-    k_attn3<<<1024, 256, 0, stream>>>(Q, K4, V4, attno);
-    k_wo<<<NN*DM/256, 256, 0, stream>>>(attno, wo + (size_t)l*128*128, bo + l*128, node);
+    if (l < 3){
+      int lp = l + 1;
+      k_qp<<<NE/32 + NN*384/256, 256, 0, stream>>>(
+          node, wqkv + (size_t)l*128*384, bqkv + l*384, Q, K4, V4,
+          edge, lw1h + (size_t)lp*32768, A16, Bm16);
+      k_la<<<1024 + NL/32, 256, 0, stream>>>(
+          Q, K4, V4, attno,
+          A16, Bm16, lsrc2, ldst2,
+          lub1 + lp*128, lw2h + (size_t)lp*16384, lub2 + lp*128,
+          lng + lp*128, lnb + lp*128, line);
+      k_we<<<NE/32 + NN*DM/256, 256, 0, stream>>>(
+          ew1h + (size_t)lp*65536, eub1 + lp*256,
+          ew2h + (size_t)lp*32768, eub2 + lp*128,
+          eng + lp*128, enb + lp*128, edge, line, base1, perm2,
+          attno, wo + (size_t)l*128*128, bo + l*128, node);
+    } else {
+      k_qkv_split<<<NN*384/256, 256, 0, stream>>>(node, wqkv + (size_t)l*128*384,
+          bqkv + l*384, Q, K4, V4);
+      k_attn3<<<1024, 256, 0, stream>>>(Q, K4, V4, attno);
+      k_wo<<<NN*DM/256, 256, 0, stream>>>(attno, wo + (size_t)l*128*128, bo + l*128, node);
+    }
   }
 
   k_readout<<<1, 256, 0, stream>>>(node, row1, rob1, row2, rob2, row3, rob3, (float*)d_out);
```

New measurement: 1.747 ms. 1.05x faster.
